# Kernel tuning notes

Measured on AMD Instinct MI355X. Metric: run time of the kernel, lower is better.

The kernel has to match this reference:

```python
import jax, jax.numpy as jnp
import numpy as np

G = 4096   # num_genes
P = 4096   # num_perts
H = 64     # hidden_size
B = 4      # num_graphs
E1 = 81920 # coexpress edges
E2 = 81920 # GO edges
FF = 512   # transformer ffn
NH = 2     # attention heads
INTER, LAT = 32, 16  # VAE dims

def _bn(x, g, b, eps=1e-5):
    # BatchNorm1d in training mode: batch stats (biased var)
    m = x.mean(0); v = x.var(0)
    return (x - m) / jnp.sqrt(v + eps) * g + b

def _ln(x, g, b, eps=1e-5):
    m = x.mean(-1, keepdims=True); v = x.var(-1, keepdims=True)
    return (x - m) / jnp.sqrt(v + eps) * g + b

def _mlp2(x, w1, b1, g1, be1, w2, b2, g2, be2):
    # MLP([a,b,c]) builds Linear->BN->ReLU->Linear->BN (trailing ReLU stripped)
    h = jax.nn.relu(_bn(x @ w1.T + b1, g1, be1))
    return _bn(h @ w2.T + b2, g2, be2)

def _sgconv(x, ei, ew, w, b, n):
    # SGConv K=1: gcn_norm (self loops, symmetric norm) then linear
    src = jnp.concatenate([ei[0], jnp.arange(n)])
    dst = jnp.concatenate([ei[1], jnp.arange(n)])
    wgt = jnp.concatenate([ew, jnp.ones((n,), ew.dtype)])
    deg = jax.ops.segment_sum(wgt, dst, num_segments=n)
    dinv = jnp.where(deg > 0, 1.0 / jnp.sqrt(jnp.where(deg > 0, deg, 1.0)), 0.0)
    norm = dinv[dst] * wgt * dinv[src]
    agg = jax.ops.segment_sum(norm[:, None] * x[src], dst, num_segments=n)
    return agg @ w.T + b

def setup_inputs():
    ks = iter(jax.random.split(jax.random.key(0), 80))
    def nrm(shape, s=0.05):
        return jax.random.normal(next(ks), shape, dtype=jnp.float32) * s
    d = {}
    d['x'] = jax.random.uniform(next(ks), (B * G,), dtype=jnp.float32)
    d['pert_idx'] = jax.random.randint(next(ks), (B, 2), 0, P)
    d['mask'] = jnp.zeros((G, G), jnp.float32)
    d['ei_co'] = jax.random.randint(next(ks), (2, E1), 0, G)
    d['w_co'] = jax.random.uniform(next(ks), (E1,), dtype=jnp.float32)
    d['ei_go'] = jax.random.randint(next(ks), (2, E2), 0, P)
    d['w_go'] = jax.random.uniform(next(ks), (E2,), dtype=jnp.float32)
    d['gene_emb'] = nrm((G, H)); d['emb_pos'] = nrm((G, H)); d['pert_tbl'] = nrm((P, H))
    d['sg_co_w'] = nrm((H, H)); d['sg_co_b'] = jnp.zeros((H,))
    d['sg_go_w'] = nrm((H, H)); d['sg_go_b'] = jnp.zeros((H,))
    d['bn_emb_g'] = jnp.ones((H,)); d['bn_emb_b'] = jnp.zeros((H,))
    for pre, din, dout in [('etv2_1', H, H), ('etv2_2', H, H), ('pf_1', H, H), ('pf_2', H, H), ('rw_1', H, 2 * H), ('rw_2', 2 * H, H)]:
        d[pre + '_w'] = nrm((dout, din)); d[pre + '_b'] = jnp.zeros((dout,))
        d[pre + '_g'] = jnp.ones((dout,)); d[pre + '_be'] = jnp.zeros((dout,))
    d['bnpb_g'] = jnp.ones((H,)); d['bnpb_b'] = jnp.zeros((H,))
    d['attn_in_w'] = nrm((3 * H, H)); d['attn_in_b'] = jnp.zeros((3 * H,))
    d['attn_out_w'] = nrm((H, H)); d['attn_out_b'] = jnp.zeros((H,))
    d['ln1_g'] = jnp.ones((H,)); d['ln1_b'] = jnp.zeros((H,))
    d['ff1_w'] = nrm((FF, H)); d['ff1_b'] = jnp.zeros((FF,))
    d['ff2_w'] = nrm((H, FF)); d['ff2_b'] = jnp.zeros((H,))
    d['ln2_g'] = jnp.ones((H,)); d['ln2_b'] = jnp.zeros((H,))
    d['indv_w1'] = nrm((G, H)); d['indv_b1'] = jnp.zeros((G,))
    d['vae_e1_w'] = nrm((INTER, G)); d['vae_e1_b'] = jnp.zeros((INTER,))
    d['vae_mu_w'] = nrm((LAT, INTER)); d['vae_mu_b'] = jnp.zeros((LAT,))
    d['vae_lv_w'] = nrm((LAT, INTER)); d['vae_lv_b'] = jnp.zeros((LAT,))
    d['vae_d1_w'] = nrm((INTER, LAT)); d['vae_d1_b'] = jnp.zeros((INTER,))
    d['vae_d2_w'] = nrm((G, INTER)); d['vae_d2_b'] = jnp.zeros((G,))
    d['eps'] = jax.random.normal(next(ks), (B, LAT), dtype=jnp.float32)
    return d

def reference(x, pert_idx, mask, ei_co, w_co, ei_go, w_go, gene_emb, emb_pos, pert_tbl, sg_co_w, sg_co_b, sg_go_w, sg_go_b, bn_emb_g, bn_emb_b, etv2_1_w, etv2_1_b, etv2_1_g, etv2_1_be, etv2_2_w, etv2_2_b, etv2_2_g, etv2_2_be, pf_1_w, pf_1_b, pf_1_g, pf_1_be, pf_2_w, pf_2_b, pf_2_g, pf_2_be, rw_1_w, rw_1_b, rw_1_g, rw_1_be, rw_2_w, rw_2_b, rw_2_g, rw_2_be, bnpb_g, bnpb_b, attn_in_w, attn_in_b, attn_out_w, attn_out_b, ln1_g, ln1_b, ff1_w, ff1_b, ff2_w, ff2_b, ln2_g, ln2_b, indv_w1, indv_b1, vae_e1_w, vae_e1_b, vae_mu_w, vae_mu_b, vae_lv_w, vae_lv_b, vae_d1_w, vae_d1_b, vae_d2_w, vae_d2_b, eps):
    # gene base embedding (identical across graphs until pert fusion)
    base = jax.nn.relu(_bn(gene_emb, bn_emb_g, bn_emb_b))               # [G,H]
    pos = _sgconv(emb_pos, ei_co, w_co, sg_co_w, sg_co_b, G)            # 1 gene-GNN layer
    base = base + 0.2 * pos
    base = _mlp2(base, etv2_1_w, etv2_1_b, etv2_1_g, etv2_1_be, etv2_2_w, etv2_2_b, etv2_2_g, etv2_2_be)
    # pert embeddings propagated on GO graph
    pge = _sgconv(pert_tbl, ei_go, w_go, sg_go_w, sg_go_b, P)           # [P,H]
    # per-graph pert_track: sum of pert embeddings (all pert_idx valid)
    psum = pge[pert_idx].sum(axis=1)                                    # [B,H]
    etot = _mlp2(psum, pf_1_w, pf_1_b, pf_1_g, pf_1_be, pf_2_w, pf_2_b, pf_2_g, pf_2_be)
    base_b = base[None, :, :] + etot[:, None, :]                        # [B,G,H]
    flat = jax.nn.relu(_bn(base_b.reshape(B * G, H), bnpb_g, bnpb_b))
    out = _mlp2(flat, rw_1_w, rw_1_b, rw_1_g, rw_1_be, rw_2_w, rw_2_b, rw_2_g, rw_2_be)
    out = out.reshape(B, G, H)
    # transformer encoder layer (post-norm, relu, nhead=2), eval/no-dropout
    qkv = out @ attn_in_w.T + attn_in_b
    q, k, v = jnp.split(qkv, 3, axis=-1)
    hd = H // NH
    q = q.reshape(B, G, NH, hd); k = k.reshape(B, G, NH, hd); v = v.reshape(B, G, NH, hd)
    sc = jnp.einsum('bqhd,bkhd->bhqk', q, k) / np.float32(np.sqrt(hd)) + mask
    a = jax.nn.softmax(sc, axis=-1)
    ctx = jnp.einsum('bhqk,bkhd->bqhd', a, v).reshape(B, G, H)
    att = ctx @ attn_out_w.T + attn_out_b
    h1 = _ln(out + att, ln1_g, ln1_b)
    ff = jax.nn.relu(h1 @ ff1_w.T + ff1_b) @ ff2_w.T + ff2_b
    enc = _ln(h1 + ff, ln2_g, ln2_b)
    # per-gene linear: (enc.unsqueeze(-1)*indv_w1).sum(2)+indv_b1
    pred0 = jnp.einsum('bgh,gh->bg', enc, indv_w1) + indv_b1
    # VAE branch on raw expression
    xr = x.reshape(B, G)
    he = jax.nn.relu(xr @ vae_e1_w.T + vae_e1_b)
    mu = he @ vae_mu_w.T + vae_mu_b
    lv = he @ vae_lv_w.T + vae_lv_b
    z = mu + eps * jnp.exp(0.5 * lv)
    hdc = jax.nn.relu(z @ vae_d1_w.T + vae_d1_b)
    recon = hdc @ vae_d2_w.T + vae_d2_b
    kl = -0.5 * jnp.mean(jnp.sum(1.0 + lv - mu ** 2 - jnp.exp(lv), axis=1))
    recon = jnp.where(xr == 0, 0.0, recon)
    pred = pred0 + recon
    return (pred, kl)
```

## Files before the change

kernel.cpp:

```cpp
#include <hip/hip_runtime.h>
#include <hip/hip_bf16.h>
#include <math.h>

#define GG 4096
#define PP 4096
#define HH 64
#define BB 4
#define E1N 81920
#define E2N 81920
#define FFD 512
#define BNEPS 1e-5f
#define LOG2E 1.44269504088896341f
#define QPRE (0.17677669529663687f * LOG2E)

typedef unsigned short ushort_t;
typedef unsigned int uint_t;
using sh8 = __attribute__((ext_vector_type(8))) short;
using sh4 = __attribute__((ext_vector_type(4))) short;
using f4  = __attribute__((ext_vector_type(4))) float;

#if __has_builtin(__builtin_amdgcn_mfma_f32_16x16x16bf16_1k)
#define MFMA16(a, b, c) __builtin_amdgcn_mfma_f32_16x16x16bf16_1k((a), (b), (c), 0, 0, 0)
#elif __has_builtin(__builtin_amdgcn_mfma_f32_16x16x16_bf16)
#define MFMA16(a, b, c) __builtin_amdgcn_mfma_f32_16x16x16_bf16((a), (b), (c), 0, 0, 0)
#else
static __device__ inline f4 mfma16_asm(sh4 a, sh4 b, f4 c) {
    f4 d;
    asm volatile("v_mfma_f32_16x16x16_bf16 %0, %1, %2, %3"
                 : "=v"(d) : "v"(a), "v"(b), "v"(c));
    return d;
}
#define MFMA16(a, b, c) mfma16_asm((a), (b), (c))
#endif

#define OF_STATS   0
#define OF_DEGCO   2048
#define OF_DEGGO   6144
#define OF_PSLOT   10240
#define OF_ETOT    10752
#define OF_HDC     11008
#define OF_HE      11136
#define OF_AGGCO   12288
#define OF_BASEIN  274432
#define OF_Y1      536576
#define OF_Y2      798720
#define OF_FLAT    1060864
#define OF_RW1     2109440
#define OF_RW2     4206592
#define OF_OUT     5255168
#define OF_QKV     6303744
#define OF_H1      10498048
#define OF_QB      OF_AGGCO
#define OF_KB      (OF_AGGCO + 524288)
#define OF_VF      OF_FLAT
#define OF_OPA     OF_QKV
#define OF_OPB     OF_OUT
#define OF_LP      OF_RW1
#define OPS        1048576
#define OF_W1B     9449472
#define OF_W2B     9465856
#define OF_H1B     9482240
#define OF_FFT     OF_FLAT

#define AGGBLKS 1024

__device__ inline ushort_t f2b(float f) {
    uint_t u = __builtin_bit_cast(uint_t, f);
    u += 0x7FFFu + ((u >> 16) & 1u);
    return (ushort_t)(u >> 16);
}

__device__ inline void gld16(const void* gptr, void* lptr) {
    __builtin_amdgcn_global_load_lds(
        (const __attribute__((address_space(1))) uint_t*)gptr,
        (__attribute__((address_space(3))) uint_t*)lptr, 16, 0, 0);
}

__device__ void dev_vae_he(int bid, const float* __restrict__ x, const float* __restrict__ W,
                           const float* __restrict__ bias, float* he, float* sh) {
    int b = bid >> 5, i = bid & 31;
    float s = 0.f;
    for (int g = threadIdx.x; g < 4096; g += 256) s += x[b * 4096 + g] * W[i * 4096 + g];
    sh[threadIdx.x] = s;
    __syncthreads();
    for (int o = 128; o > 0; o >>= 1) {
        if (threadIdx.x < o) sh[threadIdx.x] += sh[threadIdx.x + o];
        __syncthreads();
    }
    if (threadIdx.x == 0) he[b * 32 + i] = fmaxf(sh[0] + bias[i], 0.f);
}

__device__ void dev_vae_mid(const float* __restrict__ he,
                            const float* __restrict__ muw, const float* __restrict__ mub,
                            const float* __restrict__ lvw, const float* __restrict__ lvb,
                            const float* __restrict__ d1w, const float* __restrict__ d1b,
                            const float* __restrict__ eps, float* hdc, float* klout, float* zs) {
    int t = threadIdx.x;
    if (t < 64) {
        int b = t >> 4, l = t & 15;
        float mu = mub[l], lv = lvb[l];
        for (int i = 0; i < 32; i++) {
            float hv = he[b * 32 + i];
            mu += hv * muw[l * 32 + i];
            lv += hv * lvw[l * 32 + i];
        }
        zs[t] = mu + eps[t] * expf(0.5f * lv);
        float kterm = 1.f + lv - mu * mu - expf(lv);
        for (int o = 32; o > 0; o >>= 1) kterm += __shfl_xor(kterm, o, 64);
        if (t == 0) klout[0] = -0.5f * kterm * 0.25f;
    }
    __syncthreads();
    if (t < 128) {
        int b = t >> 5, i = t & 31;
        float a = d1b[i];
        for (int l = 0; l < 16; l++) a += zs[b * 16 + l] * d1w[i * 16 + l];
        hdc[t] = fmaxf(a, 0.f);
    }
}

__device__ void dev_edge_deg(int bid, const int* __restrict__ ei, const float* __restrict__ w,
                             float* deg, int E) {
    int e = bid * 256 + threadIdx.x;
    if (e < E) atomicAdd(&deg[ei[E + e]], w[e]);
}

__device__ void dev_cs_part(int bid, const float* __restrict__ X, int N,
                            float* sum, float* sumsq, float* sh) {
    int t = threadIdx.x;
    int col = t & 63, ro = t >> 6;
    int rows = N >> 8;
    int r0 = bid * rows;
    float s = 0.f, q = 0.f;
    for (int r = r0 + ro; r < r0 + rows; r += 4) {
        float v = X[r * 64 + col];
        s += v; q += v * v;
    }
    float* ls = sh; float* lq = sh + 256;
    ls[t] = s; lq[t] = q;
    __syncthreads();
    if (t < 64) {
        for (int j = t + 64; j < 256; j += 64) { s += ls[j]; q += lq[j]; }
        atomicAdd(&sum[t], s);
        atomicAdd(&sumsq[t], q);
    }
}

__device__ void dev_edge_agg(int bid, const int* __restrict__ ei, const float* __restrict__ w,
                             const float* __restrict__ deg, const float* __restrict__ x,
                             float* agg) {
    const int h = threadIdx.x & 63;
    const int wid = bid * 4 + (threadIdx.x >> 6);
    const int nw4 = AGGBLKS * 4 * 4;
    for (int e0 = wid * 4; e0 < E1N; e0 += nw4) {
        int srcs[4], dsts[4];
        float norms[4];
        #pragma unroll
        for (int j = 0; j < 4; j++) {
            int e = e0 + j;
            srcs[j] = ei[e];
            dsts[j] = ei[E1N + e];
            norms[j] = rsqrtf(deg[dsts[j]]) * w[e] * rsqrtf(deg[srcs[j]]);
        }
        float xv[4];
        #pragma unroll
        for (int j = 0; j < 4; j++) xv[j] = x[srcs[j] * HH + h];
        #pragma unroll
        for (int j = 0; j < 4; j++)
            atomicAdd(&agg[dsts[j] * HH + h], norms[j] * xv[j]);
    }
}

__device__ void dev_pert_edges(int bid, const int* __restrict__ pidx, const int* __restrict__ ei,
                               const float* __restrict__ w, const float* __restrict__ deg,
                               const float* __restrict__ tbl, float* pslot) {
    int e = bid * 256 + threadIdx.x;
    if (e >= E2N) return;
    int dst = ei[E2N + e];
    int src = ei[e];
    for (int s = 0; s < 8; s++) {
        if (pidx[s] == dst) {
            float norm = rsqrtf(deg[dst]) * w[e] * rsqrtf(deg[src]);
            for (int h = 0; h < 64; h++)
                atomicAdd(&pslot[s * 64 + h], norm * tbl[src * 64 + h]);
        }
    }
}

__device__ void dev_base_combine(int bid, const float* __restrict__ gene_emb,
                                 const float* __restrict__ agg, const float* __restrict__ emb_pos,
                                 const float* __restrict__ deg,
                                 const float* __restrict__ W, const float* __restrict__ bias,
                                 const float* __restrict__ bsum, const float* __restrict__ bsq,
                                 const float* __restrict__ bg, const float* __restrict__ bb,
                                 float* out, float* sh) {
    float* Wt = sh;
    float* a = sh + 4160;
    int t = threadIdx.x;
    for (int i = t; i < 4096; i += 256) Wt[(i & 63) * 65 + (i >> 6)] = W[i];
    int rr = t >> 6, h = t & 63;
    int g = bid * 4 + rr;
    a[rr * 64 + h] = agg[g * 64 + h] + emb_pos[g * 64 + h] / deg[g];
    __syncthreads();
    float y = bias[h];
    const float* ar = a + rr * 64;
    #pragma unroll 8
    for (int k = 0; k < 64; k++) y += ar[k] * Wt[k * 65 + h];
    const float invN = 1.0f / (float)GG;
    float m = bsum[h] * invN;
    float is_ = rsqrtf(bsq[h] * invN - m * m + BNEPS);
    float v = gene_emb[g * 64 + h];
    v = (v - m) * is_ * bg[h] + bb[h];
    v = fmaxf(v, 0.f);
    out[g * 64 + h] = v + 0.2f * y;
}

__device__ void dev_pert_mlp(const float* __restrict__ pslot, const int* __restrict__ pidx,
                             const float* __restrict__ deg, const float* __restrict__ tbl,
                             const float* __restrict__ gw, const float* __restrict__ gb,
                             const float* __restrict__ w1, const float* __restrict__ b1,
                             const float* __restrict__ g1, const float* __restrict__ be1,
                             const float* __restrict__ w2, const float* __restrict__ b2,
                             const float* __restrict__ g2, const float* __restrict__ be2,
                             float* etot, float* sh) {
    float* pge = sh;
    float* psum = sh + 512;
    float* y = sh + 768;
    float* mh = sh + 1024;
    float* ih = sh + 1088;
    int t = threadIdx.x;
    for (int j = t; j < 512; j += 256) {
        int s = j >> 6, h = j & 63;
        int n = pidx[s];
        float invd = 1.0f / deg[n];
        float acc = gb[h];
        for (int k = 0; k < 64; k++)
            acc += (pslot[s * 64 + k] + tbl[n * 64 + k] * invd) * gw[h * 64 + k];
        pge[j] = acc;
    }
    __syncthreads();
    { int b = t >> 6, h = t & 63; psum[t] = pge[2 * b * 64 + h] + pge[(2 * b + 1) * 64 + h]; }
    __syncthreads();
    { int h = t & 63; int b = t >> 6;
      float acc = b1[h];
      for (int k = 0; k < 64; k++) acc += psum[b * 64 + k] * w1[h * 64 + k];
      y[t] = acc; }
    __syncthreads();
    if (t < 64) {
        float s = 0.f, sq = 0.f;
        for (int b = 0; b < 4; b++) { float v = y[b * 64 + t]; s += v; sq += v * v; }
        float m = s * 0.25f;
        mh[t] = m; ih[t] = rsqrtf(sq * 0.25f - m * m + BNEPS);
    }
    __syncthreads();
    { int h = t & 63;
      float v = (y[t] - mh[h]) * ih[h] * g1[h] + be1[h];
      psum[t] = fmaxf(v, 0.f); }
    __syncthreads();
    { int h = t & 63; int b = t >> 6;
      float acc = b2[h];
      for (int k = 0; k < 64; k++) acc += psum[b * 64 + k] * w2[h * 64 + k];
      y[t] = acc; }
    __syncthreads();
    if (t < 64) {
        float s = 0.f, sq = 0.f;
        for (int b = 0; b < 4; b++) { float v = y[b * 64 + t]; s += v; sq += v * v; }
        float m = s * 0.25f;
        mh[t] = m; ih[t] = rsqrtf(sq * 0.25f - m * m + BNEPS);
    }
    __syncthreads();
    { int h = t & 63;
      etot[t] = (y[t] - mh[h]) * ih[h] * g2[h] + be2[h]; }
}

__global__ void k_fat1(float* ws, const float* __restrict__ x,
                       const float* __restrict__ ve1_w, const float* __restrict__ ve1_b,
                       const float* __restrict__ ff1_w, const float* __restrict__ ff2_w) {
    __shared__ float sh[256];
    const float4 z4 = {0.f, 0.f, 0.f, 0.f};
    const float4 o4 = {1.f, 1.f, 1.f, 1.f};
    int bid = blockIdx.x;
    if (bid < 256) {
        int i = bid * 256 + threadIdx.x;
        *(float4*)&ws[OF_AGGCO + i * 4] = z4;
    } else if (bid < 259) {
        int i = (bid - 256) * 256 + threadIdx.x;
        if (i < 512) *(float4*)&ws[OF_STATS + i * 4] = z4;
        else if (i < 640) *(float4*)&ws[OF_PSLOT + (i - 512) * 4] = z4;
    } else if (bid < 267) {
        int i = (bid - 259) * 256 + threadIdx.x;
        *(float4*)&ws[OF_DEGCO + i * 4] = o4;
    } else if (bid < 395) {
        dev_vae_he(bid - 267, x, ve1_w, ve1_b, ws + OF_HE, sh);
    } else {
        int i = (bid - 395) * 256 + threadIdx.x;
        ushort_t* W1b = (ushort_t*)(ws + OF_W1B);
        ushort_t* W2b = (ushort_t*)(ws + OF_W2B);
        if (i < 32768) W1b[i] = f2b(ff1_w[i]);
        else W2b[i - 32768] = f2b(ff2_w[i - 32768]);
    }
}

__global__ void k_fat2(float* ws, const int* __restrict__ ei_co, const float* __restrict__ w_co,
                       const int* __restrict__ ei_go, const float* __restrict__ w_go,
                       const float* __restrict__ gene_emb,
                       const float* __restrict__ vmu_w, const float* __restrict__ vmu_b,
                       const float* __restrict__ vlv_w, const float* __restrict__ vlv_b,
                       const float* __restrict__ vd1_w, const float* __restrict__ vd1_b,
                       const float* __restrict__ veps, float* klout) {
    __shared__ float sh[512];
    int bid = blockIdx.x;
    if (bid < 320) dev_edge_deg(bid, ei_co, w_co, ws + OF_DEGCO, E1N);
    else if (bid < 640) dev_edge_deg(bid - 320, ei_go, w_go, ws + OF_DEGGO, E2N);
    else if (bid < 896) dev_cs_part(bid - 640, gene_emb, GG, ws + OF_STATS, ws + OF_STATS + 128, sh);
    else dev_vae_mid(ws + OF_HE, vmu_w, vmu_b, vlv_w, vlv_b, vd1_w, vd1_b, veps,
                     ws + OF_HDC, klout, sh);
}

__global__ void k_fat3(float* ws, const int* __restrict__ ei_co, const float* __restrict__ w_co,
                       const float* __restrict__ emb_pos, const int* __restrict__ pidx,
                       const int* __restrict__ ei_go, const float* __restrict__ w_go,
                       const float* __restrict__ pert_tbl) {
    int bid = blockIdx.x;
    if (bid < AGGBLKS) dev_edge_agg(bid, ei_co, w_co, ws + OF_DEGCO, emb_pos, ws + OF_AGGCO);
    else dev_pert_edges(bid - AGGBLKS, pidx, ei_go, w_go, ws + OF_DEGGO, pert_tbl, ws + OF_PSLOT);
}

__global__ void k_fat4(float* ws, const float* __restrict__ gene_emb,
                       const float* __restrict__ emb_pos,
                       const float* __restrict__ sg_co_w, const float* __restrict__ sg_co_b,
                       const float* __restrict__ bn_emb_g, const float* __restrict__ bn_emb_b,
                       const int* __restrict__ pidx, const float* __restrict__ pert_tbl,
                       const float* __restrict__ gw, const float* __restrict__ gb,
                       const float* __restrict__ w1, const float* __restrict__ b1,
                       const float* __restrict__ g1, const float* __restrict__ be1,
                       const float* __restrict__ w2, const float* __restrict__ b2,
                       const float* __restrict__ g2, const float* __restrict__ be2) {
    __shared__ float sh[4416];
    int bid = blockIdx.x;
    if (bid < 1024)
        dev_base_combine(bid, gene_emb, ws + OF_AGGCO, emb_pos, ws + OF_DEGCO,
                         sg_co_w, sg_co_b, ws + OF_STATS, ws + OF_STATS + 128,
                         bn_emb_g, bn_emb_b, ws + OF_BASEIN, sh);
    else
        dev_pert_mlp(ws + OF_PSLOT, pidx, ws + OF_DEGGO, pert_tbl, gw, gb,
                     w1, b1, g1, be1, w2, b2, g2, be2, ws + OF_ETOT, sh);
}

__launch_bounds__(256)
__global__ void k_gemm64(const float* __restrict__ X, const float* __restrict__ W,
                         const float* __restrict__ bias, float* __restrict__ Y,
                         int Cin, int Cout,
                         const float* __restrict__ bnsum, const float* __restrict__ bnsq,
                         const float* __restrict__ bng, const float* __restrict__ bnb,
                         float invN, int relu_in,
                         float* __restrict__ outsum, float* __restrict__ outsq) {
    __shared__ float Xs[64][66];
    __shared__ float Ws[64][66];
    __shared__ float bsc[64], bsh[64];
    const int t = threadIdx.x;
    const int row0 = blockIdx.x * 64, cb = blockIdx.y * 64;
    const int tx = t & 15, ty = t >> 4;
    const int c0 = tx * 4, r0 = ty * 4;
    float acc[4][4];
    #pragma unroll
    for (int j = 0; j < 4; j++)
        #pragma unroll
        for (int i = 0; i < 4; i++) acc[j][i] = 0.f;

    for (int k0 = 0; k0 < Cin; k0 += 64) {
        __syncthreads();
        if (t < 64) {
            float sc = 1.f, sh = 0.f;
            if (bnsum) {
                int c = k0 + t;
                float m = bnsum[c] * invN;
                float is_ = rsqrtf(bnsq[c] * invN - m * m + BNEPS);
                sc = is_ * bng[c]; sh = bnb[c] - m * sc;
            }
            bsc[t] = sc; bsh[t] = sh;
        }
        __syncthreads();
        for (int i = t; i < 1024; i += 256) {
            int r = i >> 4, kq = (i & 15) * 4;
            float4 v = *(const float4*)&X[(size_t)(row0 + r) * Cin + k0 + kq];
            float e0 = v.x * bsc[kq] + bsh[kq];
            float e1 = v.y * bsc[kq + 1] + bsh[kq + 1];
            float e2 = v.z * bsc[kq + 2] + bsh[kq + 2];
            float e3 = v.w * bsc[kq + 3] + bsh[kq + 3];
            if (relu_in) {
                e0 = fmaxf(e0, 0.f); e1 = fmaxf(e1, 0.f);
                e2 = fmaxf(e2, 0.f); e3 = fmaxf(e3, 0.f);
            }
            Xs[r][kq] = e0; Xs[r][kq + 1] = e1; Xs[r][kq + 2] = e2; Xs[r][kq + 3] = e3;
            float4 wv = *(const float4*)&W[(size_t)(cb + r) * Cin + k0 + kq];
            Ws[r][kq] = wv.x; Ws[r][kq + 1] = wv.y; Ws[r][kq + 2] = wv.z; Ws[r][kq + 3] = wv.w;
        }
        __syncthreads();
        #pragma unroll 4
        for (int k = 0; k < 64; k += 2) {
            float2 a[4], b[4];
            #pragma unroll
            for (int j = 0; j < 4; j++) a[j] = *(const float2*)&Xs[r0 + j][k];
            #pragma unroll
            for (int i = 0; i < 4; i++) b[i] = *(const float2*)&Ws[c0 + i][k];
            #pragma unroll
            for (int j = 0; j < 4; j++)
                #pragma unroll
                for (int i = 0; i < 4; i++)
                    acc[j][i] += a[j].x * b[i].x + a[j].y * b[i].y;
        }
    }
    float4 bi = *(const float4*)&bias[cb + c0];
    float scol[4] = {0.f, 0.f, 0.f, 0.f}, qcol[4] = {0.f, 0.f, 0.f, 0.f};
    #pragma unroll
    for (int j = 0; j < 4; j++) {
        float4 o;
        o.x = acc[j][0] + bi.x; o.y = acc[j][1] + bi.y;
        o.z = acc[j][2] + bi.z; o.w = acc[j][3] + bi.w;
        *(float4*)&Y[(size_t)(row0 + r0 + j) * Cout + cb + c0] = o;
        scol[0] += o.x; scol[1] += o.y; scol[2] += o.z; scol[3] += o.w;
        qcol[0] += o.x * o.x; qcol[1] += o.y * o.y;
        qcol[2] += o.z * o.z; qcol[3] += o.w * o.w;
    }
    if (outsum) {
        __syncthreads();
        #pragma unroll
        for (int i = 0; i < 4; i++) { Xs[ty][c0 + i] = scol[i]; Ws[ty][c0 + i] = qcol[i]; }
        __syncthreads();
        if (t < 64) {
            float ss = 0.f, qq = 0.f;
            #pragma unroll
            for (int r = 0; r < 16; r++) { ss += Xs[r][t]; qq += Ws[r][t]; }
            atomicAdd(&outsum[cb + t], ss);
            atomicAdd(&outsq[cb + t], qq);
        }
    }
}

__launch_bounds__(256)
__global__ void k_gemm_qkv(const float* __restrict__ X, const float* __restrict__ W,
                           const float* __restrict__ bias,
                           const float* __restrict__ bnsum, const float* __restrict__ bnsq,
                           const float* __restrict__ bng, const float* __restrict__ bnb,
                           ushort_t* __restrict__ Qb, ushort_t* __restrict__ Kb,
                           ushort_t* __restrict__ Vf) {
    __shared__ float Xs[64][66];
    __shared__ float Ws[64][66];
    __shared__ float bsc[64], bsh[64];
    const int t = threadIdx.x;
    const int row0 = blockIdx.x * 64, yb = blockIdx.y, cb = yb * 64;
    const int tx = t & 15, ty = t >> 4;
    const int c0 = tx * 4, r0 = ty * 4;
    const float invN = 1.0f / (float)(BB * GG);
    if (t < 64) {
        float m = bnsum[t] * invN;
        float is_ = rsqrtf(bnsq[t] * invN - m * m + BNEPS);
        float sc = is_ * bng[t];
        bsc[t] = sc; bsh[t] = bnb[t] - m * sc;
    }
    __syncthreads();
    for (int i = t; i < 1024; i += 256) {
        int r = i >> 4, kq = (i & 15) * 4;
        float4 v = *(const float4*)&X[(size_t)(row0 + r) * 64 + kq];
        Xs[r][kq] = v.x * bsc[kq] + bsh[kq];
        Xs[r][kq + 1] = v.y * bsc[kq + 1] + bsh[kq + 1];
        Xs[r][kq + 2] = v.z * bsc[kq + 2] + bsh[kq + 2];
        Xs[r][kq + 3] = v.w * bsc[kq + 3] + bsh[kq + 3];
        float4 wv = *(const float4*)&W[(size_t)(cb + r) * 64 + kq];
        Ws[r][kq] = wv.x; Ws[r][kq + 1] = wv.y; Ws[r][kq + 2] = wv.z; Ws[r][kq + 3] = wv.w;
    }
    __syncthreads();
    float acc[4][4];
    #pragma unroll
    for (int j = 0; j < 4; j++)
        #pragma unroll
        for (int i = 0; i < 4; i++) acc[j][i] = 0.f;
    #pragma unroll 4
    for (int k = 0; k < 64; k += 2) {
        float2 a[4], b[4];
        #pragma unroll
        for (int j = 0; j < 4; j++) a[j] = *(const float2*)&Xs[r0 + j][k];
        #pragma unroll
        for (int i = 0; i < 4; i++) b[i] = *(const float2*)&Ws[c0 + i][k];
        #pragma unroll
        for (int j = 0; j < 4; j++)
            #pragma unroll
            for (int i = 0; i < 4; i++)
                acc[j][i] += a[j].x * b[i].x + a[j].y * b[i].y;
    }
    float4 bi = *(const float4*)&bias[cb + c0];
    const int b2 = row0 >> 12, tile = (row0 & 4095) >> 6;
    if (yb < 2) {
        ushort_t* Dst = (yb == 0) ? Qb : Kb;
        const float sc2 = (yb == 0) ? QPRE : 1.0f;
        const int h = c0 >> 5, d = c0 & 31;
        #pragma unroll
        for (int j = 0; j < 4; j++) {
            union { ushort_t u[4]; uint2 v; } pk;
            pk.u[0] = f2b((acc[j][0] + bi.x) * sc2);
            pk.u[1] = f2b((acc[j][1] + bi.y) * sc2);
            pk.u[2] = f2b((acc[j][2] + bi.z) * sc2);
            pk.u[3] = f2b((acc[j][3] + bi.w) * sc2);
            int g = (row0 & 4095) + r0 + j;
            *(uint2*)&Dst[((size_t)(b2 * 2 + h) * GG + g) * 32 + d] = pk.v;
        }
    } else {
        __syncthreads();
        #pragma unroll
        for (int j = 0; j < 4; j++) {
            Xs[r0 + j][c0] = acc[j][0] + bi.x;
            Xs[r0 + j][c0 + 1] = acc[j][1] + bi.y;
            Xs[r0 + j][c0 + 2] = acc[j][2] + bi.z;
            Xs[r0 + j][c0 + 3] = acc[j][3] + bi.w;
        }
        __syncthreads();
        #pragma unroll
        for (int h = 0; h < 2; h++) {
            union { ushort_t u[8]; uint4 v; } pk;
            #pragma unroll
            for (int j = 0; j < 8; j++) {
                int idx = t * 8 + j;
                int g2 = idx >> 8, L = (idx >> 2) & 63, i = idx & 3;
                int key = (g2 >> 1) * 16 + ((L >> 4) << 2) + i;
                int d = ((g2 & 1) << 4) + (L & 15);
                pk.u[j] = f2b(Xs[key][h * 32 + d]);
            }
            *(uint4*)&Vf[((size_t)((b2 * 2 + h) * 64 + tile)) * 2048 + t * 8] = pk.v;
        }
    }
}

__global__ void k_flatpre(const float* __restrict__ y2, const float* __restrict__ etot,
                          const float* __restrict__ bsum, const float* __restrict__ bsq,
                          const float* __restrict__ g2, const float* __restrict__ b2,
                          float* __restrict__ out,
                          float* __restrict__ osum, float* __restrict__ osq) {
    int t = threadIdx.x;
    int h = t & 63, ro = t >> 6;
    int row0 = blockIdx.x * 64;
    const float invN = 1.0f / (float)GG;
    float m = bsum[h] * invN;
    float is_ = rsqrtf(bsq[h] * invN - m * m + BNEPS);
    float sc = is_ * g2[h];
    float sh = b2[h] - m * sc;
    float s = 0.f, q = 0.f;
    for (int r = row0 + ro; r < row0 + 64; r += 4) {
        int b = r >> 12, gh = (r & 4095) * 64 + h;
        float v = y2[gh] * sc + sh + etot[b * 64 + h];
        out[r * 64 + h] = v;
        s += v; q += v * v;
    }
    __shared__ float ls[256], lq[256];
    ls[t] = s; lq[t] = q;
    __syncthreads();
    if (t < 64) {
        s = ls[t] + ls[t + 64] + ls[t + 128] + ls[t + 192];
        q = lq[t] + lq[t + 64] + lq[t + 128] + lq[t + 192];
        atomicAdd(&osum[t], s);
        atomicAdd(&osq[t], q);
    }
}

__launch_bounds__(512, 4)
__global__ void k_attn_mfma(const ushort_t* __restrict__ Qb, const ushort_t* __restrict__ Kb,
                            const ushort_t* __restrict__ Vf, const float* __restrict__ mask,
                            float* __restrict__ opA, float* __restrict__ opB,
                            float* __restrict__ Lp) {
    __shared__ ushort_t Kl[2][4][2048];
    __shared__ ushort_t Vl[2][4][2048];
    const int split = blockIdx.y;
    const int bh0 = blockIdx.z * 4;
    const int q0 = blockIdx.x * 64;
    const int kstart = split * (GG / 4), kend = kstart + (GG / 4);
    const int t = threadIdx.x;
    const int lane = t & 63, w = t >> 6;
    const int qg = w >> 1, kh = w & 1;
    const int l15 = lane & 15, quad = lane >> 4;
    const int i2a = kh * 2, i2b = kh * 2 + 1;

    sh8 qf[4];
    #pragma unroll
    for (int bh = 0; bh < 4; bh++)
        qf[bh] = *(const sh8*)&Qb[((size_t)(bh0 + bh) * GG + q0 + qg * 16 + l15) * 32 + quad * 8];
    const float* mrow = mask + (size_t)(q0 + qg * 16 + l15) * GG + quad * 4;

    auto stage = [&](int buf, int k0) {
        #pragma unroll
        for (int s = 0; s < 2; s++) {
            int idx = s * 512 + t;
            int bh = idx >> 8, c = idx & 255;
            int key = ((c >> 6) << 4) + (c & 15);
            int chunk = (c >> 4) & 3;
            gld16(Kb + ((size_t)(bh0 + bh) * GG + k0 + key) * 32 + chunk * 8,
                  &Kl[buf][bh][c * 8]);
            gld16(Vf + ((size_t)((bh0 + bh) * 64 + (k0 >> 6))) * 2048 + c * 8,
                  &Vl[buf][bh][c * 8]);
        }
    };
    stage(0, kstart);

    f4 O0[4], O1[4];
    float ls[4];
    #pragma unroll
    for (int bh = 0; bh < 4; bh++) {
        O0[bh] = f4{0.f, 0.f, 0.f, 0.f};
        O1[bh] = f4{0.f, 0.f, 0.f, 0.f};
        ls[bh] = 0.f;
    }

    for (int k0 = kstart; k0 < kend; k0 += 64) {
        const int cur = ((k0 - kstart) >> 6) & 1;
        __syncthreads();
        if (k0 + 64 < kend) stage(cur ^ 1, k0 + 64);
        float4 mva = *(const float4*)&mrow[k0 + i2a * 16];
        float4 mvb = *(const float4*)&mrow[k0 + i2b * 16];
        #pragma unroll
        for (int bh = 0; bh < 4; bh++) {
            sh8 kfa = *(const sh8*)&Kl[cur][bh][(i2a * 64 + lane) * 8];
            sh8 kfb = *(const sh8*)&Kl[cur][bh][(i2b * 64 + lane) * 8];
            f4 z = {0.f, 0.f, 0.f, 0.f};
            f4 sa = __builtin_amdgcn_mfma_f32_16x16x32_bf16(kfa, qf[bh], z, 0, 0, 0);
            f4 sb = __builtin_amdgcn_mfma_f32_16x16x32_bf16(kfb, qf[bh], z, 0, 0, 0);
            {
                float p0 = exp2f(fmaf(mva.x, LOG2E, sa[0]));
                float p1 = exp2f(fmaf(mva.y, LOG2E, sa[1]));
                float p2 = exp2f(fmaf(mva.z, LOG2E, sa[2]));
                float p3 = exp2f(fmaf(mva.w, LOG2E, sa[3]));
                ls[bh] += (p0 + p1) + (p2 + p3);
                union { __hip_bfloat162 h2[2]; sh4 v; } pkp;
                pkp.h2[0] = __float22bfloat162_rn(float2{p0, p1});
                pkp.h2[1] = __float22bfloat162_rn(float2{p2, p3});
                sh4 vf0 = *(const sh4*)&Vl[cur][bh][((i2a * 2 + 0) * 64 + lane) * 4];
                sh4 vf1 = *(const sh4*)&Vl[cur][bh][((i2a * 2 + 1) * 64 + lane) * 4];
                O0[bh] = MFMA16(pkp.v, vf0, O0[bh]);
                O1[bh] = MFMA16(pkp.v, vf1, O1[bh]);
            }
            {
                float p0 = exp2f(fmaf(mvb.x, LOG2E, sb[0]));
                float p1 = exp2f(fmaf(mvb.y, LOG2E, sb[1]));
                float p2 = exp2f(fmaf(mvb.z, LOG2E, sb[2]));
                float p3 = exp2f(fmaf(mvb.w, LOG2E, sb[3]));
                ls[bh] += (p0 + p1) + (p2 + p3);
                union { __hip_bfloat162 h2[2]; sh4 v; } pkp;
                pkp.h2[0] = __float22bfloat162_rn(float2{p0, p1});
                pkp.h2[1] = __float22bfloat162_rn(float2{p2, p3});
                sh4 vf0 = *(const sh4*)&Vl[cur][bh][((i2b * 2 + 0) * 64 + lane) * 4];
                sh4 vf1 = *(const sh4*)&Vl[cur][bh][((i2b * 2 + 1) * 64 + lane) * 4];
                O0[bh] = MFMA16(pkp.v, vf0, O0[bh]);
                O1[bh] = MFMA16(pkp.v, vf1, O1[bh]);
            }
        }
    }
    #pragma unroll
    for (int bh = 0; bh < 4; bh++) {
        ls[bh] += __shfl_xor(ls[bh], 16, 64);
        ls[bh] += __shfl_xor(ls[bh], 32, 64);
    }
    __syncthreads();
    float* Ox = (float*)&Kl[0][0][0];
    float* Lx = (float*)&Vl[0][0][0];
    if (kh == 0) {
        #pragma unroll
        for (int bh = 0; bh < 4; bh++) {
            #pragma unroll
            for (int r = 0; r < 4; r++) {
                int ql = qg * 16 + quad * 4 + r;
                Ox[(bh * 64 + ql) * 32 + l15] = O0[bh][r];
                Ox[(bh * 64 + ql) * 32 + l15 + 16] = O1[bh][r];
            }
            if (quad == 0) Lx[bh * 64 + qg * 16 + l15] = ls[bh];
        }
    }
    __syncthreads();
    if (kh == 1) {
        float* op = (split < 3) ? (opA + (size_t)split * OPS) : opB;
        #pragma unroll
        for (int bh = 0; bh < 4; bh++) {
            int gbh = bh0 + bh;
            #pragma unroll
            for (int r = 0; r < 4; r++) {
                int ql = qg * 16 + quad * 4 + r;
                size_t o = ((size_t)gbh * GG + q0 + ql) * 32 + l15;
                op[o] = O0[bh][r] + Ox[(bh * 64 + ql) * 32 + l15];
                op[o + 16] = O1[bh][r] + Ox[(bh * 64 + ql) * 32 + l15 + 16];
            }
            if (quad == 0)
                Lp[split * 32768 + gbh * GG + q0 + qg * 16 + l15] =
                    ls[bh] + Lx[bh * 64 + qg * 16 + l15];
        }
    }
}

__global__ void k_attn_out_ln(const float* __restrict__ opA, const float* __restrict__ opB,
                              const float* __restrict__ Lp, const float* __restrict__ yrw2,
                              const float* __restrict__ W, const float* __restrict__ bias,
                              const float* __restrict__ bsum, const float* __restrict__ bsq,
                              const float* __restrict__ bg, const float* __restrict__ bb,
                              const float* __restrict__ lg, const float* __restrict__ lb,
                              float* __restrict__ h1, ushort_t* __restrict__ h1b) {
    __shared__ float Wt[64][65];
    __shared__ float Cs[16][65];
    __shared__ ushort_t Hs[16][64];
    int t = threadIdx.x;
    int row0 = blockIdx.x * 16;
    for (int i = t; i < 4096; i += 256) Wt[i & 63][i >> 6] = W[i];
    {
        int col = t & 63, rl = t >> 6;
        int hh = col >> 5, d = col & 31;
        #pragma unroll
        for (int jj = 0; jj < 4; jj++) {
            int row = row0 + rl + jj * 4;
            int b = row >> 12, q = row & 4095;
            int bhq = (b * 2 + hh) * GG + q;
            size_t oi = (size_t)bhq * 32 + d;
            float num = opA[oi] + opA[OPS + oi] + opA[2 * OPS + oi] + opB[oi];
            float den = Lp[bhq] + Lp[32768 + bhq] + Lp[65536 + bhq] + Lp[98304 + bhq];
            Cs[rl + jj * 4][col] = num / den;
        }
    }
    __syncthreads();
    int rr = t >> 6, lane = t & 63;
    const float invN = 1.0f / (float)(BB * GG);
    float m = bsum[lane] * invN;
    float is_ = rsqrtf(bsq[lane] * invN - m * m + BNEPS);
    #pragma unroll
    for (int j = 0; j < 4; j++) {
        int lrow = rr * 4 + j;
        int row = row0 + lrow;
        float acc = bias[lane];
        const float* cr = Cs[lrow];
        #pragma unroll 8
        for (int k = 0; k < 64; k++) acc += cr[k] * Wt[k][lane];
        float ov = (yrw2[row * 64 + lane] - m) * is_ * bg[lane] + bb[lane];
        float v = ov + acc;
        float s = v;
        for (int o = 32; o > 0; o >>= 1) s += __shfl_xor(s, o, 64);
        float mean = s * (1.f / 64.f);
        float d = v - mean;
        float sq = d * d;
        for (int o = 32; o > 0; o >>= 1) sq += __shfl_xor(sq, o, 64);
        float inv = rsqrtf(sq * (1.f / 64.f) + BNEPS);
        float hv = d * inv * lg[lane] + lb[lane];
        h1[row * 64 + lane] = hv;
        Hs[lrow][lane] = f2b(hv);
    }
    __syncthreads();
    if (t < 128) {
        int kt = t >> 6, lane6 = t & 63;
        int q2 = (lane6 >> 4) & 3, r15 = lane6 & 15;
        union { ushort_t u[8]; uint4 v; } pk;
        #pragma unroll
        for (int j = 0; j < 8; j++) pk.u[j] = Hs[r15][kt * 32 + q2 * 8 + j];
        *(uint4*)&h1b[((size_t)blockIdx.x * 2 + kt) * 512 + lane6 * 8] = pk.v;
    }
}

__launch_bounds__(256)
__global__ void k_ffn1(const ushort_t* __restrict__ h1b, const ushort_t* __restrict__ W1b,
                       const float* __restrict__ b1, ushort_t* __restrict__ fft) {
    __shared__ ushort_t Xl[4096];
    __shared__ ushort_t Wl[4096];
    const int t = threadIdx.x;
    const int rowblock = blockIdx.x, colblock = blockIdx.y;
    const int cb = colblock * 64;
    const int lane = t & 63, w = t >> 6;
    const int l15 = lane & 15, quad = lane >> 4;
    #pragma unroll
    for (int kt = 0; kt < 2; kt++) {
        gld16(h1b + (size_t)(((rowblock * 4 + w) * 2 + kt) * 512 + lane * 8),
              &Xl[(w * 2 + kt) * 512 + lane * 8]);
        gld16(W1b + (size_t)((cb + w * 16 + l15) * 64 + kt * 32 + quad * 8),
              &Wl[(w * 2 + kt) * 512 + lane * 8]);
    }
    __syncthreads();
    sh8 xf0 = *(const sh8*)&Xl[(w * 2 + 0) * 512 + lane * 8];
    sh8 xf1 = *(const sh8*)&Xl[(w * 2 + 1) * 512 + lane * 8];
    #pragma unroll
    for (int c = 0; c < 4; c++) {
        sh8 wf0 = *(const sh8*)&Wl[(c * 2 + 0) * 512 + lane * 8];
        sh8 wf1 = *(const sh8*)&Wl[(c * 2 + 1) * 512 + lane * 8];
        f4 z = {0.f, 0.f, 0.f, 0.f};
        f4 acc = __builtin_amdgcn_mfma_f32_16x16x32_bf16(wf0, xf0, z, 0, 0, 0);
        acc = __builtin_amdgcn_mfma_f32_16x16x32_bf16(wf1, xf1, acc, 0, 0, 0);
        float4 bv = *(const float4*)&b1[cb + c * 16 + quad * 4];
        union { ushort_t u[4]; uint2 v; } pk;
        pk.u[0] = f2b(fmaxf(acc[0] + bv.x, 0.f));
        pk.u[1] = f2b(fmaxf(acc[1] + bv.y, 0.f));
        pk.u[2] = f2b(fmaxf(acc[2] + bv.z, 0.f));
        pk.u[3] = f2b(fmaxf(acc[3] + bv.w, 0.f));
        int kt512 = colblock * 2 + (c >> 1);
        int quadp = (c & 1) * 2 + (quad >> 1);
        int j0 = (quad & 1) * 4;
        size_t o = ((size_t)(((rowblock * 4 + w) * 16 + kt512) * 64 + quadp * 16 + l15)) * 8 + j0;
        *(uint2*)&fft[o] = pk.v;
    }
}

__launch_bounds__(256)
__global__ void k_ffn2(const ushort_t* __restrict__ fft, const ushort_t* __restrict__ W2b,
                       const float* __restrict__ b2, const float* __restrict__ h1,
                       const float* __restrict__ lg, const float* __restrict__ lb,
                       const float* __restrict__ indvw, const float* __restrict__ indvb,
                       const float* __restrict__ hdc, const float* __restrict__ d2w,
                       const float* __restrict__ d2b, const float* __restrict__ x,
                       float* __restrict__ outp) {
    __shared__ ushort_t Xl[2][4096];
    __shared__ ushort_t Wl[2][4096];
    const int t = threadIdx.x;
    const int rowblock = blockIdx.x;
    const int lane = t & 63, w = t >> 6;
    const int l15 = lane & 15, quad = lane >> 4;

    #pragma unroll
    for (int kt = 0; kt < 2; kt++) {
        gld16(fft + (size_t)((((rowblock * 4 + w) * 16) + kt) * 64 + lane) * 8,
              &Xl[0][(w * 2 + kt) * 512 + lane * 8]);
        gld16(W2b + (size_t)((w * 16 + l15) * 512 + kt * 32 + quad * 8),
              &Wl[0][(w * 2 + kt) * 512 + lane * 8]);
    }
    f4 acc[4];
    #pragma unroll
    for (int c = 0; c < 4; c++) acc[c] = f4{0.f, 0.f, 0.f, 0.f};

    for (int k0 = 0; k0 < 512; k0 += 64) {
        const int cur = (k0 >> 6) & 1;
        __syncthreads();
        if (k0 + 64 < 512) {
            const int nxt = cur ^ 1;
            const int ktb = (k0 + 64) >> 5;
            #pragma unroll
            for (int kt = 0; kt < 2; kt++) {
                gld16(fft + (size_t)((((rowblock * 4 + w) * 16) + ktb + kt) * 64 + lane) * 8,
                      &Xl[nxt][(w * 2 + kt) * 512 + lane * 8]);
                gld16(W2b + (size_t)((w * 16 + l15) * 512 + k0 + 64 + kt * 32 + quad * 8),
                      &Wl[nxt][(w * 2 + kt) * 512 + lane * 8]);
            }
        }
        #pragma unroll
        for (int kt = 0; kt < 2; kt++) {
            sh8 xf = *(const sh8*)&Xl[cur][(w * 2 + kt) * 512 + lane * 8];
            #pragma unroll
            for (int c = 0; c < 4; c++) {
                sh8 wf = *(const sh8*)&Wl[cur][(c * 2 + kt) * 512 + lane * 8];
                acc[c] = __builtin_amdgcn_mfma_f32_16x16x32_bf16(wf, xf, acc[c], 0, 0, 0);
            }
        }
    }
    const int row = rowblock * 64 + w * 16 + l15;
    const int b = row >> 12, g = row & 4095;
    float v[4][4];
    float s = 0.f, sq = 0.f;
    #pragma unroll
    for (int c = 0; c < 4; c++) {
        float4 bv = *(const float4*)&b2[c * 16 + quad * 4];
        float4 hv = *(const float4*)&h1[(size_t)row * 64 + c * 16 + quad * 4];
        v[c][0] = hv.x + acc[c][0] + bv.x;
        v[c][1] = hv.y + acc[c][1] + bv.y;
        v[c][2] = hv.z + acc[c][2] + bv.z;
        v[c][3] = hv.w + acc[c][3] + bv.w;
        #pragma unroll
        for (int i = 0; i < 4; i++) { s += v[c][i]; sq += v[c][i] * v[c][i]; }
    }
    s += __shfl_xor(s, 16, 64);  s += __shfl_xor(s, 32, 64);
    sq += __shfl_xor(sq, 16, 64); sq += __shfl_xor(sq, 32, 64);
    float mean = s * (1.f / 64.f);
    float inv = rsqrtf(sq * (1.f / 64.f) - mean * mean + BNEPS);
    float pd = 0.f;
    #pragma unroll
    for (int c = 0; c < 4; c++) {
        float4 lgv = *(const float4*)&lg[c * 16 + quad * 4];
        float4 lbv = *(const float4*)&lb[c * 16 + quad * 4];
        float4 iwv = *(const float4*)&indvw[(size_t)g * 64 + c * 16 + quad * 4];
        pd += ((v[c][0] - mean) * inv * lgv.x + lbv.x) * iwv.x;
        pd += ((v[c][1] - mean) * inv * lgv.y + lbv.y) * iwv.y;
        pd += ((v[c][2] - mean) * inv * lgv.z + lbv.z) * iwv.z;
        pd += ((v[c][3] - mean) * inv * lgv.w + lbv.w) * iwv.w;
    }
    float rc = 0.f;
    #pragma unroll
    for (int i = 0; i < 8; i++)
        rc += hdc[b * 32 + quad * 8 + i] * d2w[(size_t)g * 32 + quad * 8 + i];
    pd += __shfl_xor(pd, 16, 64); pd += __shfl_xor(pd, 32, 64);
    rc += __shfl_xor(rc, 16, 64); rc += __shfl_xor(rc, 32, 64);
    if (quad == 0) {
        float recon = rc + d2b[g];
        if (x[row] == 0.f) recon = 0.f;
        outp[row] = pd + indvb[g] + recon;
    }
}

extern "C" void kernel_launch(void* const* d_in, const int* in_sizes, int n_in,
                              void* d_out, int out_size, void* d_ws, size_t ws_size,
                              hipStream_t stream) {
    const float* x        = (const float*)d_in[0];
    const int*   pert_idx = (const int*)  d_in[1];
    const float* mask     = (const float*)d_in[2];
    const int*   ei_co    = (const int*)  d_in[3];
    const float* w_co     = (const float*)d_in[4];
    const int*   ei_go    = (const int*)  d_in[5];
    const float* w_go     = (const float*)d_in[6];
    const float* gene_emb = (const float*)d_in[7];
    const float* emb_pos  = (const float*)d_in[8];
    const float* pert_tbl = (const float*)d_in[9];
    const float* sg_co_w  = (const float*)d_in[10];
    const float* sg_co_b  = (const float*)d_in[11];
    const float* sg_go_w  = (const float*)d_in[12];
    const float* sg_go_b  = (const float*)d_in[13];
    const float* bn_emb_g = (const float*)d_in[14];
    const float* bn_emb_b = (const float*)d_in[15];
    const float* etv1_w   = (const float*)d_in[16];
    const float* etv1_b   = (const float*)d_in[17];
    const float* etv1_g   = (const float*)d_in[18];
    const float* etv1_be  = (const float*)d_in[19];
    const float* etv2_w   = (const float*)d_in[20];
    const float* etv2_b   = (const float*)d_in[21];
    const float* etv2_g   = (const float*)d_in[22];
    const float* etv2_be  = (const float*)d_in[23];
    const float* pf1_w    = (const float*)d_in[24];
    const float* pf1_b    = (const float*)d_in[25];
    const float* pf1_g    = (const float*)d_in[26];
    const float* pf1_be   = (const float*)d_in[27];
    const float* pf2_w    = (const float*)d_in[28];
    const float* pf2_b    = (const float*)d_in[29];
    const float* pf2_g    = (const float*)d_in[30];
    const float* pf2_be   = (const float*)d_in[31];
    const float* rw1_w    = (const float*)d_in[32];
    const float* rw1_b    = (const float*)d_in[33];
    const float* rw1_g    = (const float*)d_in[34];
    const float* rw1_be   = (const float*)d_in[35];
    const float* rw2_w    = (const float*)d_in[36];
    const float* rw2_b    = (const float*)d_in[37];
    const float* rw2_g    = (const float*)d_in[38];
    const float* rw2_be   = (const float*)d_in[39];
    const float* bnpb_g   = (const float*)d_in[40];
    const float* bnpb_b   = (const float*)d_in[41];
    const float* ain_w    = (const float*)d_in[42];
    const float* ain_b    = (const float*)d_in[43];
    const float* aout_w   = (const float*)d_in[44];
    const float* aout_b   = (const float*)d_in[45];
    const float* ln1_g    = (const float*)d_in[46];
    const float* ln1_b    = (const float*)d_in[47];
    const float* ff1_w    = (const float*)d_in[48];
    const float* ff1_b    = (const float*)d_in[49];
    const float* ff2_w    = (const float*)d_in[50];
    const float* ff2_b    = (const float*)d_in[51];
    const float* ln2_g    = (const float*)d_in[52];
    const float* ln2_b    = (const float*)d_in[53];
    const float* indv_w   = (const float*)d_in[54];
    const float* indv_b   = (const float*)d_in[55];
    const float* ve1_w    = (const float*)d_in[56];
    const float* ve1_b    = (const float*)d_in[57];
    const float* vmu_w    = (const float*)d_in[58];
    const float* vmu_b    = (const float*)d_in[59];
    const float* vlv_w    = (const float*)d_in[60];
    const float* vlv_b    = (const float*)d_in[61];
    const float* vd1_w    = (const float*)d_in[62];
    const float* vd1_b    = (const float*)d_in[63];
    const float* vd2_w    = (const float*)d_in[64];
    const float* vd2_b    = (const float*)d_in[65];
    const float* veps     = (const float*)d_in[66];

    float* ws   = (float*)d_ws;
    float* outp = (float*)d_out;

    float* stm1 = ws + OF_STATS + 1 * 256; float* sti1 = stm1 + 128;
    float* stm2 = ws + OF_STATS + 2 * 256; float* sti2 = stm2 + 128;
    float* stm3 = ws + OF_STATS + 3 * 256; float* sti3 = stm3 + 128;
    float* stm4 = ws + OF_STATS + 4 * 256; float* sti4 = stm4 + 128;
    float* stm5 = ws + OF_STATS + 5 * 256; float* sti5 = stm5 + 128;

    float* basein = ws + OF_BASEIN;
    float* y1     = ws + OF_Y1;
    float* y2     = ws + OF_Y2;
    float* flat   = ws + OF_FLAT;
    float* yrw1   = ws + OF_RW1;
    float* yrw2   = ws + OF_RW2;
    float* h1     = ws + OF_H1;
    float* opA    = ws + OF_OPA;
    float* opB    = ws + OF_OPB;
    float* Lp     = ws + OF_LP;
    ushort_t* Qb  = (ushort_t*)(ws + OF_QB);
    ushort_t* Kb  = (ushort_t*)(ws + OF_KB);
    ushort_t* Vf  = (ushort_t*)(ws + OF_VF);
    ushort_t* W1b = (ushort_t*)(ws + OF_W1B);
    ushort_t* W2b = (ushort_t*)(ws + OF_W2B);
    ushort_t* h1b = (ushort_t*)(ws + OF_H1B);
    ushort_t* fft = (ushort_t*)(ws + OF_FFT);

    const int NG = BB * GG;
    const float iG = 1.0f / (float)GG, iNG = 1.0f / (float)NG;

    k_fat1<<<651, 256, 0, stream>>>(ws, x, ve1_w, ve1_b, ff1_w, ff2_w);
    k_fat2<<<897, 256, 0, stream>>>(ws, ei_co, w_co, ei_go, w_go, gene_emb,
                                    vmu_w, vmu_b, vlv_w, vlv_b, vd1_w, vd1_b,
                                    veps, outp + NG);
    k_fat3<<<AGGBLKS + 320, 256, 0, stream>>>(ws, ei_co, w_co, emb_pos, pert_idx,
                                              ei_go, w_go, pert_tbl);
    k_fat4<<<1025, 256, 0, stream>>>(ws, gene_emb, emb_pos, sg_co_w, sg_co_b,
                                     bn_emb_g, bn_emb_b, pert_idx, pert_tbl,
                                     sg_go_w, sg_go_b,
                                     pf1_w, pf1_b, pf1_g, pf1_be,
                                     pf2_w, pf2_b, pf2_g, pf2_be);
    k_gemm64<<<dim3(GG / 64, 1), 256, 0, stream>>>(basein, etv1_w, etv1_b, y1, 64, 64,
                                                   nullptr, nullptr, nullptr, nullptr, 0.f, 0,
                                                   stm1, sti1);
    k_gemm64<<<dim3(GG / 64, 1), 256, 0, stream>>>(y1, etv2_w, etv2_b, y2, 64, 64,
                                                   stm1, sti1, etv1_g, etv1_be, iG, 1,
                                                   stm2, sti2);
    k_flatpre<<<NG / 64, 256, 0, stream>>>(y2, ws + OF_ETOT, stm2, sti2, etv2_g, etv2_be,
                                           flat, stm3, sti3);
    k_gemm64<<<dim3(NG / 64, 2), 256, 0, stream>>>(flat, rw1_w, rw1_b, yrw1, 64, 128,
                                                   stm3, sti3, bnpb_g, bnpb_b, iNG, 1,
                                                   stm4, sti4);
    k_gemm64<<<dim3(NG / 64, 1), 256, 0, stream>>>(yrw1, rw2_w, rw2_b, yrw2, 128, 64,
                                                   stm4, sti4, rw1_g, rw1_be, iNG, 1,
                                                   stm5, sti5);
    k_gemm_qkv<<<dim3(NG / 64, 3), 256, 0, stream>>>(yrw2, ain_w, ain_b,
                                                     stm5, sti5, rw2_g, rw2_be,
                                                     Qb, Kb, Vf);
    k_attn_mfma<<<dim3(GG / 64, 4, 2), 512, 0, stream>>>(Qb, Kb, Vf, mask, opA, opB, Lp);
    k_attn_out_ln<<<NG / 16, 256, 0, stream>>>(opA, opB, Lp, yrw2, aout_w, aout_b,
                                               stm5, sti5, rw2_g, rw2_be,
                                               ln1_g, ln1_b, h1, h1b);
    k_ffn1<<<dim3(NG / 64, FFD / 64), 256, 0, stream>>>(h1b, W1b, ff1_b, fft);
    k_ffn2<<<NG / 64, 256, 0, stream>>>(fft, W2b, ff2_b, h1, ln2_g, ln2_b,
                                        indv_w, indv_b, ws + OF_HDC, vd2_w, vd2_b,
                                        x, outp);
}
```

Before: 522.7 us.

## Fuse launch chain: merge fat kernels, fold flatpre BN into rw1 GEMM, fuse attention-out/FFN tail

Replaces the zero-initialization kernel with hipMemsetAsync and merges the degree, stats and VAE-encoder phases into one launch. The VAE middle stage moves into the edge-aggregation launch. The degree buffer is no longer preset to one, so the self-loop +1 is added at each use. The separate flatten/BN pass is removed: its statistics are derived analytically from the previous BN sums and the etot offsets inside a new rw1 GEMM. Attention-output projection, LayerNorm1, FFN1, FFN2 and the output stage are fused into one k_tail kernel that keeps h1 and the FFN intermediate in LDS. This removes several launches and global round-trips, at the cost of much larger LDS use per block and lower occupancy in the tail.

```diff
diff --git a/kernel.cpp b/kernel.cpp
--- a/kernel.cpp
+++ b/kernel.cpp
@@ -49,7 +49,6 @@
 #define OF_RW2     4206592
 #define OF_OUT     5255168
 #define OF_QKV     6303744
-#define OF_H1      10498048
 #define OF_QB      OF_AGGCO
 #define OF_KB      (OF_AGGCO + 524288)
 #define OF_VF      OF_FLAT
@@ -59,8 +58,6 @@
 #define OPS        1048576
 #define OF_W1B     9449472
 #define OF_W2B     9465856
-#define OF_H1B     9482240
-#define OF_FFT     OF_FLAT
 
 #define AGGBLKS 1024
 
@@ -159,7 +156,7 @@
             int e = e0 + j;
             srcs[j] = ei[e];
             dsts[j] = ei[E1N + e];
-            norms[j] = rsqrtf(deg[dsts[j]]) * w[e] * rsqrtf(deg[srcs[j]]);
+            norms[j] = rsqrtf(deg[dsts[j]] + 1.f) * w[e] * rsqrtf(deg[srcs[j]] + 1.f);
         }
         float xv[4];
         #pragma unroll
@@ -179,7 +176,7 @@
     int src = ei[e];
     for (int s = 0; s < 8; s++) {
         if (pidx[s] == dst) {
-            float norm = rsqrtf(deg[dst]) * w[e] * rsqrtf(deg[src]);
+            float norm = rsqrtf(deg[dst] + 1.f) * w[e] * rsqrtf(deg[src] + 1.f);
             for (int h = 0; h < 64; h++)
                 atomicAdd(&pslot[s * 64 + h], norm * tbl[src * 64 + h]);
         }
@@ -199,7 +196,7 @@
     for (int i = t; i < 4096; i += 256) Wt[(i & 63) * 65 + (i >> 6)] = W[i];
     int rr = t >> 6, h = t & 63;
     int g = bid * 4 + rr;
-    a[rr * 64 + h] = agg[g * 64 + h] + emb_pos[g * 64 + h] / deg[g];
+    a[rr * 64 + h] = agg[g * 64 + h] + emb_pos[g * 64 + h] / (deg[g] + 1.f);
     __syncthreads();
     float y = bias[h];
     const float* ar = a + rr * 64;
@@ -231,7 +228,7 @@
     for (int j = t; j < 512; j += 256) {
         int s = j >> 6, h = j & 63;
         int n = pidx[s];
-        float invd = 1.0f / deg[n];
+        float invd = 1.0f / (deg[n] + 1.f);
         float acc = gb[h];
         for (int k = 0; k < 64; k++)
             acc += (pslot[s * 64 + k] + tbl[n * 64 + k] * invd) * gw[h * 64 + k];
@@ -272,27 +269,19 @@
       etot[t] = (y[t] - mh[h]) * ih[h] * g2[h] + be2[h]; }
 }
 
-__global__ void k_fat1(float* ws, const float* __restrict__ x,
-                       const float* __restrict__ ve1_w, const float* __restrict__ ve1_b,
-                       const float* __restrict__ ff1_w, const float* __restrict__ ff2_w) {
-    __shared__ float sh[256];
-    const float4 z4 = {0.f, 0.f, 0.f, 0.f};
-    const float4 o4 = {1.f, 1.f, 1.f, 1.f};
+__global__ void k_fat12(float* ws, const int* __restrict__ ei_co, const float* __restrict__ w_co,
+                        const int* __restrict__ ei_go, const float* __restrict__ w_go,
+                        const float* __restrict__ gene_emb, const float* __restrict__ x,
+                        const float* __restrict__ ve1_w, const float* __restrict__ ve1_b,
+                        const float* __restrict__ ff1_w, const float* __restrict__ ff2_w) {
+    __shared__ float sh[512];
     int bid = blockIdx.x;
-    if (bid < 256) {
-        int i = bid * 256 + threadIdx.x;
-        *(float4*)&ws[OF_AGGCO + i * 4] = z4;
-    } else if (bid < 259) {
-        int i = (bid - 256) * 256 + threadIdx.x;
-        if (i < 512) *(float4*)&ws[OF_STATS + i * 4] = z4;
-        else if (i < 640) *(float4*)&ws[OF_PSLOT + (i - 512) * 4] = z4;
-    } else if (bid < 267) {
-        int i = (bid - 259) * 256 + threadIdx.x;
-        *(float4*)&ws[OF_DEGCO + i * 4] = o4;
-    } else if (bid < 395) {
-        dev_vae_he(bid - 267, x, ve1_w, ve1_b, ws + OF_HE, sh);
-    } else {
-        int i = (bid - 395) * 256 + threadIdx.x;
+    if (bid < 320) dev_edge_deg(bid, ei_co, w_co, ws + OF_DEGCO, E1N);
+    else if (bid < 640) dev_edge_deg(bid - 320, ei_go, w_go, ws + OF_DEGGO, E2N);
+    else if (bid < 896) dev_cs_part(bid - 640, gene_emb, GG, ws + OF_STATS, ws + OF_STATS + 128, sh);
+    else if (bid < 1024) dev_vae_he(bid - 896, x, ve1_w, ve1_b, ws + OF_HE, sh);
+    else {
+        int i = (bid - 1024) * 256 + threadIdx.x;
         ushort_t* W1b = (ushort_t*)(ws + OF_W1B);
         ushort_t* W2b = (ushort_t*)(ws + OF_W2B);
         if (i < 32768) W1b[i] = f2b(ff1_w[i]);
@@ -300,29 +289,21 @@
     }
 }
 
-__global__ void k_fat2(float* ws, const int* __restrict__ ei_co, const float* __restrict__ w_co,
+__global__ void k_fat3(float* ws, const int* __restrict__ ei_co, const float* __restrict__ w_co,
+                       const float* __restrict__ emb_pos, const int* __restrict__ pidx,
                        const int* __restrict__ ei_go, const float* __restrict__ w_go,
-                       const float* __restrict__ gene_emb,
+                       const float* __restrict__ pert_tbl,
                        const float* __restrict__ vmu_w, const float* __restrict__ vmu_b,
                        const float* __restrict__ vlv_w, const float* __restrict__ vlv_b,
                        const float* __restrict__ vd1_w, const float* __restrict__ vd1_b,
                        const float* __restrict__ veps, float* klout) {
     __shared__ float sh[512];
     int bid = blockIdx.x;
-    if (bid < 320) dev_edge_deg(bid, ei_co, w_co, ws + OF_DEGCO, E1N);
-    else if (bid < 640) dev_edge_deg(bid - 320, ei_go, w_go, ws + OF_DEGGO, E2N);
-    else if (bid < 896) dev_cs_part(bid - 640, gene_emb, GG, ws + OF_STATS, ws + OF_STATS + 128, sh);
+    if (bid < AGGBLKS) dev_edge_agg(bid, ei_co, w_co, ws + OF_DEGCO, emb_pos, ws + OF_AGGCO);
+    else if (bid < AGGBLKS + 320)
+        dev_pert_edges(bid - AGGBLKS, pidx, ei_go, w_go, ws + OF_DEGGO, pert_tbl, ws + OF_PSLOT);
     else dev_vae_mid(ws + OF_HE, vmu_w, vmu_b, vlv_w, vlv_b, vd1_w, vd1_b, veps,
                      ws + OF_HDC, klout, sh);
-}
-
-__global__ void k_fat3(float* ws, const int* __restrict__ ei_co, const float* __restrict__ w_co,
-                       const float* __restrict__ emb_pos, const int* __restrict__ pidx,
-                       const int* __restrict__ ei_go, const float* __restrict__ w_go,
-                       const float* __restrict__ pert_tbl) {
-    int bid = blockIdx.x;
-    if (bid < AGGBLKS) dev_edge_agg(bid, ei_co, w_co, ws + OF_DEGCO, emb_pos, ws + OF_AGGCO);
-    else dev_pert_edges(bid - AGGBLKS, pidx, ei_go, w_go, ws + OF_DEGGO, pert_tbl, ws + OF_PSLOT);
 }
 
 __global__ void k_fat4(float* ws, const float* __restrict__ gene_emb,
@@ -434,6 +415,97 @@
             atomicAdd(&outsum[cb + t], ss);
             atomicAdd(&outsq[cb + t], qq);
         }
+    }
+}
+
+__launch_bounds__(256)
+__global__ void k_gemm_rw1(const float* __restrict__ y2, const float* __restrict__ etot,
+                           const float* __restrict__ s2sum, const float* __restrict__ s2sq,
+                           const float* __restrict__ g2e, const float* __restrict__ b2e,
+                           const float* __restrict__ g3, const float* __restrict__ b3,
+                           const float* __restrict__ W, const float* __restrict__ bias,
+                           float* __restrict__ Y,
+                           float* __restrict__ osum, float* __restrict__ osq) {
+    __shared__ float Xs[64][66];
+    __shared__ float Ws[64][66];
+    __shared__ float bsc[64], bsh[64];
+    const int t = threadIdx.x;
+    const int row0 = blockIdx.x * 64, cb = blockIdx.y * 64;
+    const int tx = t & 15, ty = t >> 4;
+    const int c0 = tx * 4, r0 = ty * 4;
+    const int bb = row0 >> 12;
+    if (t < 64) {
+        const float iG = 1.0f / 4096.f, iNG = 1.0f / 16384.f;
+        float S1 = s2sum[t], S2 = s2sq[t];
+        float m2 = S1 * iG;
+        float is2 = rsqrtf(S2 * iG - m2 * m2 + BNEPS);
+        float sc2 = is2 * g2e[t], sh2 = b2e[t] - m2 * sc2;
+        float sz = sc2 * S1 + 4096.f * sh2;
+        float szz = sc2 * sc2 * S2 + 2.f * sc2 * sh2 * S1 + 4096.f * sh2 * sh2;
+        float e0 = etot[t], e1 = etot[64 + t], e2 = etot[128 + t], e3 = etot[192 + t];
+        float se = e0 + e1 + e2 + e3;
+        float see = e0 * e0 + e1 * e1 + e2 * e2 + e3 * e3;
+        float sumF = 4.f * sz + 4096.f * se;
+        float sqF = 4.f * szz + 2.f * sz * se + 4096.f * see;
+        float m3 = sumF * iNG;
+        float is3 = rsqrtf(sqF * iNG - m3 * m3 + BNEPS);
+        float eb = etot[bb * 64 + t];
+        bsc[t] = sc2 * is3 * g3[t];
+        bsh[t] = (sh2 + eb - m3) * is3 * g3[t] + b3[t];
+    }
+    __syncthreads();
+    for (int i = t; i < 1024; i += 256) {
+        int r = i >> 4, kq = (i & 15) * 4;
+        int g = (row0 + r) & 4095;
+        float4 v = *(const float4*)&y2[(size_t)g * 64 + kq];
+        Xs[r][kq] = fmaxf(v.x * bsc[kq] + bsh[kq], 0.f);
+        Xs[r][kq + 1] = fmaxf(v.y * bsc[kq + 1] + bsh[kq + 1], 0.f);
+        Xs[r][kq + 2] = fmaxf(v.z * bsc[kq + 2] + bsh[kq + 2], 0.f);
+        Xs[r][kq + 3] = fmaxf(v.w * bsc[kq + 3] + bsh[kq + 3], 0.f);
+        float4 wv = *(const float4*)&W[(size_t)(cb + r) * 64 + kq];
+        Ws[r][kq] = wv.x; Ws[r][kq + 1] = wv.y; Ws[r][kq + 2] = wv.z; Ws[r][kq + 3] = wv.w;
+    }
+    __syncthreads();
+    float acc[4][4];
+    #pragma unroll
+    for (int j = 0; j < 4; j++)
+        #pragma unroll
+        for (int i = 0; i < 4; i++) acc[j][i] = 0.f;
+    #pragma unroll 4
+    for (int k = 0; k < 64; k += 2) {
+        float2 a[4], b[4];
+        #pragma unroll
+        for (int j = 0; j < 4; j++) a[j] = *(const float2*)&Xs[r0 + j][k];
+        #pragma unroll
+        for (int i = 0; i < 4; i++) b[i] = *(const float2*)&Ws[c0 + i][k];
+        #pragma unroll
+        for (int j = 0; j < 4; j++)
+            #pragma unroll
+            for (int i = 0; i < 4; i++)
+                acc[j][i] += a[j].x * b[i].x + a[j].y * b[i].y;
+    }
+    float4 bi = *(const float4*)&bias[cb + c0];
+    float scol[4] = {0.f, 0.f, 0.f, 0.f}, qcol[4] = {0.f, 0.f, 0.f, 0.f};
+    #pragma unroll
+    for (int j = 0; j < 4; j++) {
+        float4 o;
+        o.x = acc[j][0] + bi.x; o.y = acc[j][1] + bi.y;
+        o.z = acc[j][2] + bi.z; o.w = acc[j][3] + bi.w;
+        *(float4*)&Y[(size_t)(row0 + r0 + j) * 128 + cb + c0] = o;
+        scol[0] += o.x; scol[1] += o.y; scol[2] += o.z; scol[3] += o.w;
+        qcol[0] += o.x * o.x; qcol[1] += o.y * o.y;
+        qcol[2] += o.z * o.z; qcol[3] += o.w * o.w;
+    }
+    __syncthreads();
+    #pragma unroll
+    for (int i = 0; i < 4; i++) { Xs[ty][c0 + i] = scol[i]; Ws[ty][c0 + i] = qcol[i]; }
+    __syncthreads();
+    if (t < 64) {
+        float ss = 0.f, qq = 0.f;
+        #pragma unroll
+        for (int r = 0; r < 16; r++) { ss += Xs[r][t]; qq += Ws[r][t]; }
+        atomicAdd(&osum[cb + t], ss);
+        atomicAdd(&osq[cb + t], qq);
     }
 }
 
@@ -527,37 +599,6 @@
             }
             *(uint4*)&Vf[((size_t)((b2 * 2 + h) * 64 + tile)) * 2048 + t * 8] = pk.v;
         }
-    }
-}
-
-__global__ void k_flatpre(const float* __restrict__ y2, const float* __restrict__ etot,
-                          const float* __restrict__ bsum, const float* __restrict__ bsq,
-                          const float* __restrict__ g2, const float* __restrict__ b2,
-                          float* __restrict__ out,
-                          float* __restrict__ osum, float* __restrict__ osq) {
-    int t = threadIdx.x;
-    int h = t & 63, ro = t >> 6;
-    int row0 = blockIdx.x * 64;
-    const float invN = 1.0f / (float)GG;
-    float m = bsum[h] * invN;
-    float is_ = rsqrtf(bsq[h] * invN - m * m + BNEPS);
-    float sc = is_ * g2[h];
-    float sh = b2[h] - m * sc;
-    float s = 0.f, q = 0.f;
-    for (int r = row0 + ro; r < row0 + 64; r += 4) {
-        int b = r >> 12, gh = (r & 4095) * 64 + h;
-        float v = y2[gh] * sc + sh + etot[b * 64 + h];
-        out[r * 64 + h] = v;
-        s += v; q += v * v;
-    }
-    __shared__ float ls[256], lq[256];
-    ls[t] = s; lq[t] = q;
-    __syncthreads();
-    if (t < 64) {
-        s = ls[t] + ls[t + 64] + ls[t + 128] + ls[t + 192];
-        q = lq[t] + lq[t + 64] + lq[t + 128] + lq[t + 192];
-        atomicAdd(&osum[t], s);
-        atomicAdd(&osq[t], q);
     }
 }
 
@@ -691,47 +732,58 @@
     }
 }
 
-__global__ void k_attn_out_ln(const float* __restrict__ opA, const float* __restrict__ opB,
-                              const float* __restrict__ Lp, const float* __restrict__ yrw2,
-                              const float* __restrict__ W, const float* __restrict__ bias,
-                              const float* __restrict__ bsum, const float* __restrict__ bsq,
-                              const float* __restrict__ bg, const float* __restrict__ bb,
-                              const float* __restrict__ lg, const float* __restrict__ lb,
-                              float* __restrict__ h1, ushort_t* __restrict__ h1b) {
-    __shared__ float Wt[64][65];
-    __shared__ float Cs[16][65];
-    __shared__ ushort_t Hs[16][64];
-    int t = threadIdx.x;
-    int row0 = blockIdx.x * 16;
-    for (int i = t; i < 4096; i += 256) Wt[i & 63][i >> 6] = W[i];
+__launch_bounds__(256)
+__global__ void k_tail(const float* __restrict__ opA, const float* __restrict__ opB,
+                       const float* __restrict__ Lp, const float* __restrict__ yrw2,
+                       const float* __restrict__ Waout, const float* __restrict__ baout,
+                       const float* __restrict__ bsum5, const float* __restrict__ bsq5,
+                       const float* __restrict__ bg5, const float* __restrict__ bb5,
+                       const float* __restrict__ lg1, const float* __restrict__ lb1,
+                       const ushort_t* __restrict__ W1b, const float* __restrict__ b1f,
+                       const ushort_t* __restrict__ W2b, const float* __restrict__ b2f,
+                       const float* __restrict__ lg2, const float* __restrict__ lb2,
+                       const float* __restrict__ indvw, const float* __restrict__ indvb,
+                       const float* __restrict__ hdc, const float* __restrict__ d2w,
+                       const float* __restrict__ d2b, const float* __restrict__ x,
+                       float* __restrict__ outp) {
+    __shared__ float Wt[4160];
+    __shared__ float Cs[4160];
+    __shared__ ushort_t Hb[4096];
+    __shared__ ushort_t FT[32768];
+    __shared__ ushort_t WS[2][4096];
+    const int t = threadIdx.x;
+    const int r0b = blockIdx.x * 64;
+    const int lane = t & 63, w = t >> 6;
+    const int l15 = lane & 15, quad = lane >> 4;
+
+    for (int i = t; i < 4096; i += 256) Wt[(i & 63) * 65 + (i >> 6)] = Waout[i];
     {
         int col = t & 63, rl = t >> 6;
         int hh = col >> 5, d = col & 31;
-        #pragma unroll
-        for (int jj = 0; jj < 4; jj++) {
-            int row = row0 + rl + jj * 4;
+        for (int jj = 0; jj < 16; jj++) {
+            int lrow = rl + jj * 4;
+            int row = r0b + lrow;
             int b = row >> 12, q = row & 4095;
             int bhq = (b * 2 + hh) * GG + q;
             size_t oi = (size_t)bhq * 32 + d;
             float num = opA[oi] + opA[OPS + oi] + opA[2 * OPS + oi] + opB[oi];
             float den = Lp[bhq] + Lp[32768 + bhq] + Lp[65536 + bhq] + Lp[98304 + bhq];
-            Cs[rl + jj * 4][col] = num / den;
-        }
-    }
-    __syncthreads();
-    int rr = t >> 6, lane = t & 63;
+            Cs[lrow * 65 + col] = num / den;
+        }
+    }
+    __syncthreads();
     const float invN = 1.0f / (float)(BB * GG);
-    float m = bsum[lane] * invN;
-    float is_ = rsqrtf(bsq[lane] * invN - m * m + BNEPS);
-    #pragma unroll
-    for (int j = 0; j < 4; j++) {
-        int lrow = rr * 4 + j;
-        int row = row0 + lrow;
-        float acc = bias[lane];
-        const float* cr = Cs[lrow];
+    float m5 = bsum5[lane] * invN;
+    float is5 = rsqrtf(bsq5[lane] * invN - m5 * m5 + BNEPS);
+    float h1v[16];
+    for (int j = 0; j < 16; j++) {
+        int lrow = w * 16 + j;
+        int row = r0b + lrow;
+        float acc = baout[lane];
+        const float* cr = Cs + lrow * 65;
         #pragma unroll 8
-        for (int k = 0; k < 64; k++) acc += cr[k] * Wt[k][lane];
-        float ov = (yrw2[row * 64 + lane] - m) * is_ * bg[lane] + bb[lane];
+        for (int k = 0; k < 64; k++) acc += cr[k] * Wt[k * 65 + lane];
+        float ov = (yrw2[(size_t)row * 64 + lane] - m5) * is5 * bg5[lane] + bb5[lane];
         float v = ov + acc;
         float s = v;
         for (int o = 32; o > 0; o >>= 1) s += __shfl_xor(s, o, 64);
@@ -740,126 +792,96 @@
         float sq = d * d;
         for (int o = 32; o > 0; o >>= 1) sq += __shfl_xor(sq, o, 64);
         float inv = rsqrtf(sq * (1.f / 64.f) + BNEPS);
-        float hv = d * inv * lg[lane] + lb[lane];
-        h1[row * 64 + lane] = hv;
-        Hs[lrow][lane] = f2b(hv);
-    }
+        h1v[j] = d * inv * lg1[lane] + lb1[lane];
+    }
+    __syncthreads();
+    float* h1f = Wt;
+    for (int j = 0; j < 16; j++) h1f[(w * 16 + j) * 65 + lane] = h1v[j];
     __syncthreads();
     if (t < 128) {
         int kt = t >> 6, lane6 = t & 63;
         int q2 = (lane6 >> 4) & 3, r15 = lane6 & 15;
-        union { ushort_t u[8]; uint4 v; } pk;
-        #pragma unroll
-        for (int j = 0; j < 8; j++) pk.u[j] = Hs[r15][kt * 32 + q2 * 8 + j];
-        *(uint4*)&h1b[((size_t)blockIdx.x * 2 + kt) * 512 + lane6 * 8] = pk.v;
-    }
-}
-
-__launch_bounds__(256)
-__global__ void k_ffn1(const ushort_t* __restrict__ h1b, const ushort_t* __restrict__ W1b,
-                       const float* __restrict__ b1, ushort_t* __restrict__ fft) {
-    __shared__ ushort_t Xl[4096];
-    __shared__ ushort_t Wl[4096];
-    const int t = threadIdx.x;
-    const int rowblock = blockIdx.x, colblock = blockIdx.y;
-    const int cb = colblock * 64;
-    const int lane = t & 63, w = t >> 6;
-    const int l15 = lane & 15, quad = lane >> 4;
-    #pragma unroll
-    for (int kt = 0; kt < 2; kt++) {
-        gld16(h1b + (size_t)(((rowblock * 4 + w) * 2 + kt) * 512 + lane * 8),
-              &Xl[(w * 2 + kt) * 512 + lane * 8]);
-        gld16(W1b + (size_t)((cb + w * 16 + l15) * 64 + kt * 32 + quad * 8),
-              &Wl[(w * 2 + kt) * 512 + lane * 8]);
-    }
-    __syncthreads();
-    sh8 xf0 = *(const sh8*)&Xl[(w * 2 + 0) * 512 + lane * 8];
-    sh8 xf1 = *(const sh8*)&Xl[(w * 2 + 1) * 512 + lane * 8];
-    #pragma unroll
-    for (int c = 0; c < 4; c++) {
-        sh8 wf0 = *(const sh8*)&Wl[(c * 2 + 0) * 512 + lane * 8];
-        sh8 wf1 = *(const sh8*)&Wl[(c * 2 + 1) * 512 + lane * 8];
-        f4 z = {0.f, 0.f, 0.f, 0.f};
-        f4 acc = __builtin_amdgcn_mfma_f32_16x16x32_bf16(wf0, xf0, z, 0, 0, 0);
-        acc = __builtin_amdgcn_mfma_f32_16x16x32_bf16(wf1, xf1, acc, 0, 0, 0);
-        float4 bv = *(const float4*)&b1[cb + c * 16 + quad * 4];
-        union { ushort_t u[4]; uint2 v; } pk;
-        pk.u[0] = f2b(fmaxf(acc[0] + bv.x, 0.f));
-        pk.u[1] = f2b(fmaxf(acc[1] + bv.y, 0.f));
-        pk.u[2] = f2b(fmaxf(acc[2] + bv.z, 0.f));
-        pk.u[3] = f2b(fmaxf(acc[3] + bv.w, 0.f));
-        int kt512 = colblock * 2 + (c >> 1);
-        int quadp = (c & 1) * 2 + (quad >> 1);
-        int j0 = (quad & 1) * 4;
-        size_t o = ((size_t)(((rowblock * 4 + w) * 16 + kt512) * 64 + quadp * 16 + l15)) * 8 + j0;
-        *(uint2*)&fft[o] = pk.v;
-    }
-}
-
-__launch_bounds__(256)
-__global__ void k_ffn2(const ushort_t* __restrict__ fft, const ushort_t* __restrict__ W2b,
-                       const float* __restrict__ b2, const float* __restrict__ h1,
-                       const float* __restrict__ lg, const float* __restrict__ lb,
-                       const float* __restrict__ indvw, const float* __restrict__ indvb,
-                       const float* __restrict__ hdc, const float* __restrict__ d2w,
-                       const float* __restrict__ d2b, const float* __restrict__ x,
-                       float* __restrict__ outp) {
-    __shared__ ushort_t Xl[2][4096];
-    __shared__ ushort_t Wl[2][4096];
-    const int t = threadIdx.x;
-    const int rowblock = blockIdx.x;
-    const int lane = t & 63, w = t >> 6;
-    const int l15 = lane & 15, quad = lane >> 4;
-
-    #pragma unroll
-    for (int kt = 0; kt < 2; kt++) {
-        gld16(fft + (size_t)((((rowblock * 4 + w) * 16) + kt) * 64 + lane) * 8,
-              &Xl[0][(w * 2 + kt) * 512 + lane * 8]);
-        gld16(W2b + (size_t)((w * 16 + l15) * 512 + kt * 32 + quad * 8),
-              &Wl[0][(w * 2 + kt) * 512 + lane * 8]);
-    }
-    f4 acc[4];
-    #pragma unroll
-    for (int c = 0; c < 4; c++) acc[c] = f4{0.f, 0.f, 0.f, 0.f};
-
+        for (int rg = 0; rg < 4; rg++) {
+            union { ushort_t u[8]; uint4 v4; } pk;
+            #pragma unroll
+            for (int j = 0; j < 8; j++)
+                pk.u[j] = f2b(h1f[(rg * 16 + r15) * 65 + kt * 32 + q2 * 8 + j]);
+            *(uint4*)&Hb[(rg * 2 + kt) * 512 + lane6 * 8] = pk.v4;
+        }
+    }
+    auto stage1 = [&](int buf, int cb8) {
+        int cb = cb8 * 64;
+        #pragma unroll
+        for (int kt = 0; kt < 2; kt++)
+            gld16(W1b + (size_t)((cb + w * 16 + l15) * 64 + kt * 32 + quad * 8),
+                  &WS[buf][(w * 2 + kt) * 512 + lane * 8]);
+    };
+    stage1(0, 0);
+    for (int cb8 = 0; cb8 < 8; cb8++) {
+        const int cur = cb8 & 1;
+        __syncthreads();
+        if (cb8 + 1 < 8) stage1(cur ^ 1, cb8 + 1);
+        sh8 xf0 = *(const sh8*)&Hb[(w * 2 + 0) * 512 + lane * 8];
+        sh8 xf1 = *(const sh8*)&Hb[(w * 2 + 1) * 512 + lane * 8];
+        const int cb = cb8 * 64;
+        #pragma unroll
+        for (int c = 0; c < 4; c++) {
+            sh8 wf0 = *(const sh8*)&WS[cur][(c * 2 + 0) * 512 + lane * 8];
+            sh8 wf1 = *(const sh8*)&WS[cur][(c * 2 + 1) * 512 + lane * 8];
+            f4 z = {0.f, 0.f, 0.f, 0.f};
+            f4 acc = __builtin_amdgcn_mfma_f32_16x16x32_bf16(wf0, xf0, z, 0, 0, 0);
+            acc = __builtin_amdgcn_mfma_f32_16x16x32_bf16(wf1, xf1, acc, 0, 0, 0);
+            float4 bv = *(const float4*)&b1f[cb + c * 16 + quad * 4];
+            union { ushort_t u[4]; uint2 v2; } pk;
+            pk.u[0] = f2b(fmaxf(acc[0] + bv.x, 0.f));
+            pk.u[1] = f2b(fmaxf(acc[1] + bv.y, 0.f));
+            pk.u[2] = f2b(fmaxf(acc[2] + bv.z, 0.f));
+            pk.u[3] = f2b(fmaxf(acc[3] + bv.w, 0.f));
+            int kt512 = cb8 * 2 + (c >> 1);
+            int quadp = (c & 1) * 2 + (quad >> 1);
+            int j0 = (quad & 1) * 4;
+            *(uint2*)&FT[((w * 16 + kt512) * 64 + quadp * 16 + l15) * 8 + j0] = pk.v2;
+        }
+    }
+    auto stage2 = [&](int buf, int k0) {
+        #pragma unroll
+        for (int kt = 0; kt < 2; kt++)
+            gld16(W2b + (size_t)((w * 16 + l15) * 512 + k0 + kt * 32 + quad * 8),
+                  &WS[buf][(w * 2 + kt) * 512 + lane * 8]);
+    };
+    stage2(0, 0);
+    f4 acc2[4];
+    #pragma unroll
+    for (int c = 0; c < 4; c++) acc2[c] = f4{0.f, 0.f, 0.f, 0.f};
     for (int k0 = 0; k0 < 512; k0 += 64) {
         const int cur = (k0 >> 6) & 1;
         __syncthreads();
-        if (k0 + 64 < 512) {
-            const int nxt = cur ^ 1;
-            const int ktb = (k0 + 64) >> 5;
-            #pragma unroll
-            for (int kt = 0; kt < 2; kt++) {
-                gld16(fft + (size_t)((((rowblock * 4 + w) * 16) + ktb + kt) * 64 + lane) * 8,
-                      &Xl[nxt][(w * 2 + kt) * 512 + lane * 8]);
-                gld16(W2b + (size_t)((w * 16 + l15) * 512 + k0 + 64 + kt * 32 + quad * 8),
-                      &Wl[nxt][(w * 2 + kt) * 512 + lane * 8]);
-            }
-        }
+        if (k0 + 64 < 512) stage2(cur ^ 1, k0 + 64);
+        const int ktb = k0 >> 5;
         #pragma unroll
         for (int kt = 0; kt < 2; kt++) {
-            sh8 xf = *(const sh8*)&Xl[cur][(w * 2 + kt) * 512 + lane * 8];
+            sh8 xf = *(const sh8*)&FT[((w * 16 + ktb + kt) * 64 + lane) * 8];
             #pragma unroll
             for (int c = 0; c < 4; c++) {
-                sh8 wf = *(const sh8*)&Wl[cur][(c * 2 + kt) * 512 + lane * 8];
-                acc[c] = __builtin_amdgcn_mfma_f32_16x16x32_bf16(wf, xf, acc[c], 0, 0, 0);
+                sh8 wf = *(const sh8*)&WS[cur][(c * 2 + kt) * 512 + lane * 8];
+                acc2[c] = __builtin_amdgcn_mfma_f32_16x16x32_bf16(wf, xf, acc2[c], 0, 0, 0);
             }
         }
     }
-    const int row = rowblock * 64 + w * 16 + l15;
+    const int row = r0b + w * 16 + l15;
     const int b = row >> 12, g = row & 4095;
     float v[4][4];
     float s = 0.f, sq = 0.f;
     #pragma unroll
     for (int c = 0; c < 4; c++) {
-        float4 bv = *(const float4*)&b2[c * 16 + quad * 4];
-        float4 hv = *(const float4*)&h1[(size_t)row * 64 + c * 16 + quad * 4];
-        v[c][0] = hv.x + acc[c][0] + bv.x;
-        v[c][1] = hv.y + acc[c][1] + bv.y;
-        v[c][2] = hv.z + acc[c][2] + bv.z;
-        v[c][3] = hv.w + acc[c][3] + bv.w;
-        #pragma unroll
-        for (int i = 0; i < 4; i++) { s += v[c][i]; sq += v[c][i] * v[c][i]; }
+        float4 bv = *(const float4*)&b2f[c * 16 + quad * 4];
+        #pragma unroll
+        for (int i = 0; i < 4; i++) {
+            float hv = h1f[(w * 16 + l15) * 65 + c * 16 + quad * 4 + i];
+            float bvi = (i == 0) ? bv.x : (i == 1) ? bv.y : (i == 2) ? bv.z : bv.w;
+            v[c][i] = hv + acc2[c][i] + bvi;
+            s += v[c][i]; sq += v[c][i] * v[c][i];
+        }
     }
     s += __shfl_xor(s, 16, 64);  s += __shfl_xor(s, 32, 64);
     sq += __shfl_xor(sq, 16, 64); sq += __shfl_xor(sq, 32, 64);
@@ -868,8 +890,8 @@
     float pd = 0.f;
     #pragma unroll
     for (int c = 0; c < 4; c++) {
-        float4 lgv = *(const float4*)&lg[c * 16 + quad * 4];
-        float4 lbv = *(const float4*)&lb[c * 16 + quad * 4];
+        float4 lgv = *(const float4*)&lg2[c * 16 + quad * 4];
+        float4 lbv = *(const float4*)&lb2[c * 16 + quad * 4];
         float4 iwv = *(const float4*)&indvw[(size_t)g * 64 + c * 16 + quad * 4];
         pd += ((v[c][0] - mean) * inv * lgv.x + lbv.x) * iwv.x;
         pd += ((v[c][1] - mean) * inv * lgv.y + lbv.y) * iwv.y;
@@ -965,17 +987,14 @@
 
     float* stm1 = ws + OF_STATS + 1 * 256; float* sti1 = stm1 + 128;
     float* stm2 = ws + OF_STATS + 2 * 256; float* sti2 = stm2 + 128;
-    float* stm3 = ws + OF_STATS + 3 * 256; float* sti3 = stm3 + 128;
     float* stm4 = ws + OF_STATS + 4 * 256; float* sti4 = stm4 + 128;
     float* stm5 = ws + OF_STATS + 5 * 256; float* sti5 = stm5 + 128;
 
     float* basein = ws + OF_BASEIN;
     float* y1     = ws + OF_Y1;
     float* y2     = ws + OF_Y2;
-    float* flat   = ws + OF_FLAT;
     float* yrw1   = ws + OF_RW1;
     float* yrw2   = ws + OF_RW2;
-    float* h1     = ws + OF_H1;
     float* opA    = ws + OF_OPA;
     float* opB    = ws + OF_OPB;
     float* Lp     = ws + OF_LP;
@@ -984,18 +1003,19 @@
     ushort_t* Vf  = (ushort_t*)(ws + OF_VF);
     ushort_t* W1b = (ushort_t*)(ws + OF_W1B);
     ushort_t* W2b = (ushort_t*)(ws + OF_W2B);
-    ushort_t* h1b = (ushort_t*)(ws + OF_H1B);
-    ushort_t* fft = (ushort_t*)(ws + OF_FFT);
 
     const int NG = BB * GG;
     const float iG = 1.0f / (float)GG, iNG = 1.0f / (float)NG;
 
-    k_fat1<<<651, 256, 0, stream>>>(ws, x, ve1_w, ve1_b, ff1_w, ff2_w);
-    k_fat2<<<897, 256, 0, stream>>>(ws, ei_co, w_co, ei_go, w_go, gene_emb,
-                                    vmu_w, vmu_b, vlv_w, vlv_b, vd1_w, vd1_b,
-                                    veps, outp + NG);
-    k_fat3<<<AGGBLKS + 320, 256, 0, stream>>>(ws, ei_co, w_co, emb_pos, pert_idx,
-                                              ei_go, w_go, pert_tbl);
+    hipMemsetAsync(ws, 0, 10752 * sizeof(float), stream);
+    hipMemsetAsync(ws + OF_AGGCO, 0, (size_t)GG * HH * sizeof(float), stream);
+
+    k_fat12<<<1280, 256, 0, stream>>>(ws, ei_co, w_co, ei_go, w_go, gene_emb,
+                                      x, ve1_w, ve1_b, ff1_w, ff2_w);
+    k_fat3<<<AGGBLKS + 321, 256, 0, stream>>>(ws, ei_co, w_co, emb_pos, pert_idx,
+                                              ei_go, w_go, pert_tbl,
+                                              vmu_w, vmu_b, vlv_w, vlv_b, vd1_w, vd1_b,
+                                              veps, outp + NG);
     k_fat4<<<1025, 256, 0, stream>>>(ws, gene_emb, emb_pos, sg_co_w, sg_co_b,
                                      bn_emb_g, bn_emb_b, pert_idx, pert_tbl,
                                      sg_go_w, sg_go_b,
@@ -1007,11 +1027,9 @@
     k_gemm64<<<dim3(GG / 64, 1), 256, 0, stream>>>(y1, etv2_w, etv2_b, y2, 64, 64,
                                                    stm1, sti1, etv1_g, etv1_be, iG, 1,
                                                    stm2, sti2);
-    k_flatpre<<<NG / 64, 256, 0, stream>>>(y2, ws + OF_ETOT, stm2, sti2, etv2_g, etv2_be,
-                                           flat, stm3, sti3);
-    k_gemm64<<<dim3(NG / 64, 2), 256, 0, stream>>>(flat, rw1_w, rw1_b, yrw1, 64, 128,
-                                                   stm3, sti3, bnpb_g, bnpb_b, iNG, 1,
-                                                   stm4, sti4);
+    k_gemm_rw1<<<dim3(NG / 64, 2), 256, 0, stream>>>(y2, ws + OF_ETOT, stm2, sti2,
+                                                     etv2_g, etv2_be, bnpb_g, bnpb_b,
+                                                     rw1_w, rw1_b, yrw1, stm4, sti4);
     k_gemm64<<<dim3(NG / 64, 1), 256, 0, stream>>>(yrw1, rw2_w, rw2_b, yrw2, 128, 64,
                                                    stm4, sti4, rw1_g, rw1_be, iNG, 1,
                                                    stm5, sti5);
@@ -1019,11 +1037,9 @@
                                                      stm5, sti5, rw2_g, rw2_be,
                                                      Qb, Kb, Vf);
     k_attn_mfma<<<dim3(GG / 64, 4, 2), 512, 0, stream>>>(Qb, Kb, Vf, mask, opA, opB, Lp);
-    k_attn_out_ln<<<NG / 16, 256, 0, stream>>>(opA, opB, Lp, yrw2, aout_w, aout_b,
-                                               stm5, sti5, rw2_g, rw2_be,
-                                               ln1_g, ln1_b, h1, h1b);
-    k_ffn1<<<dim3(NG / 64, FFD / 64), 256, 0, stream>>>(h1b, W1b, ff1_b, fft);
-    k_ffn2<<<NG / 64, 256, 0, stream>>>(fft, W2b, ff2_b, h1, ln2_g, ln2_b,
+    k_tail<<<NG / 64, 256, 0, stream>>>(opA, opB, Lp, yrw2, aout_w, aout_b,
+                                        stm5, sti5, rw2_g, rw2_be, ln1_g, ln1_b,
+                                        W1b, ff1_b, W2b, ff2_b, ln2_g, ln2_b,
                                         indv_w, indv_b, ws + OF_HDC, vd2_w, vd2_b,
                                         x, outp);
 }
```

Result: faster. 501.8 us (-4.0%).
